# Performance work log

Measured on AMD Instinct MI355X. Metric: run time of the kernel, lower is better.

Reference implementation:

```python
import jax, jax.numpy as jnp
import numpy as np

EPS = 1e-5
DEPTH = 3
NQ = 12


def _bn(x, g, b):
    # BatchNorm1d in training mode: batch statistics, biased variance
    mu = x.mean(0)
    var = x.var(0)
    return (x - mu) / jnp.sqrt(var + EPS) * g + b


def _ln(x, g, b):
    mu = x.mean(-1, keepdims=True)
    var = x.var(-1, keepdims=True)
    return (x - mu) / jnp.sqrt(var + EPS) * g + b


def _apply_1q(s, U, q):
    # s: [B, 2^NQ] complex; U: [2,2] (shared) or [B,2,2] (per-sample); qubit q = q-th MSB
    B = s.shape[0]
    s = s.reshape(B, 2 ** q, 2, -1)
    sub = 'ij,bajc->baic' if U.ndim == 2 else 'bij,bajc->baic'
    return jnp.einsum(sub, U, s).reshape(B, -1)


def _apply_cry(s, theta, c):
    # controlled-Ry(theta): control qubit c, target qubit c+1 (adjacent)
    B = s.shape[0]
    s = s.reshape(B, 2 ** c, 2, 2, -1)
    co = jnp.cos(theta / 2).astype(s.dtype)
    si = jnp.sin(theta / 2).astype(s.dtype)
    s1 = s[:, :, 1]  # control = |1> block
    new1 = jnp.stack([co * s1[:, :, 0] - si * s1[:, :, 1],
                      si * s1[:, :, 0] + co * s1[:, :, 1]], axis=2)
    s = jnp.concatenate([s[:, :, :1], new1[:, :, None]], axis=2)
    return s.reshape(B, -1)


def _measure(s):
    # P(qubit q measures |1>) for each qubit
    p = jnp.abs(s) ** 2  # [B, 2^NQ]
    B = p.shape[0]
    probs = [p.reshape(B, 2 ** q, 2, -1).sum(axis=(1, 3))[:, 1] for q in range(NQ)]
    return jnp.stack(probs, axis=1)  # [B, NQ]


def _rot_mats(rot):
    # fused Rz(rz) @ Ry(ry) @ Rx(rx) for each (depth, qubit) -> [DEPTH, NQ, 2, 2]
    hx, hy, hz = rot[..., 0] / 2, rot[..., 1] / 2, rot[..., 2] / 2
    cx, sx = jnp.cos(hx), jnp.sin(hx)
    Rx = jnp.stack([jnp.stack([cx + 0j, -1j * sx], -1),
                    jnp.stack([-1j * sx, cx + 0j], -1)], -2)
    cy, sy = jnp.cos(hy), jnp.sin(hy)
    Ry = jnp.stack([jnp.stack([cy, -sy], -1),
                    jnp.stack([sy, cy], -1)], -2).astype(jnp.complex64)
    ez = jnp.exp(-1j * hz)
    z0 = jnp.zeros_like(ez)
    Rz = jnp.stack([jnp.stack([ez, z0], -1),
                    jnp.stack([z0, jnp.conj(ez)], -1)], -2)
    return jnp.einsum('...ij,...jk,...kl->...il', Rz, Ry, Rx).astype(jnp.complex64)


def _quantum_layer(x, We, be, gi, bi, rot, ent, Wd, bd, go, bo):
    e = jnp.tanh(_bn(x @ We.T + be, gi, bi))  # [B, NQ]
    nrm = jnp.linalg.norm(e, axis=1, keepdims=True)
    a = jnp.where(nrm > 0, e / nrm, e)        # per-sample L2-normalized amplitudes
    B = x.shape[0]
    s = jnp.zeros((B, 2 ** NQ), jnp.complex64).at[:, 0].set(1.0)
    # amplitude encoding: Ry(2*arcsin(|a|)) then phase pi (sign) if a<0 -> diag(1,-1)@Ry
    ang = 2.0 * jnp.arcsin(jnp.clip(jnp.abs(a), 0.0, 1.0))
    c, si = jnp.cos(ang / 2), jnp.sin(ang / 2)
    sg = jnp.where(a < 0, -1.0, 1.0)
    for q in range(NQ):
        U = jnp.stack([jnp.stack([c[:, q], -si[:, q]], -1),
                       jnp.stack([sg[:, q] * si[:, q], sg[:, q] * c[:, q]], -1)],
                      -2).astype(jnp.complex64)  # [B,2,2]
        s = _apply_1q(s, U, q)
    # parameterized circuit: per-qubit fused Rz.Ry.Rx, then nearest-neighbor CRy chain
    U = _rot_mats(rot)
    for d in range(DEPTH):
        for q in range(NQ):
            s = _apply_1q(s, U[d, q], q)
        for i in range(NQ - 1):
            s = _apply_cry(s, ent[d, i], i)
    m = _measure(s)
    return _bn(m @ Wd.T + bd, go, bo)


def setup_inputs() -> dict:
    key = jax.random.key(0)
    ks = jax.random.split(key, 16)
    B, IN, H1, H2, H3, OUT = 512, 512, 512, 512, 1024, 256

    def lin(k, o, i):
        k1, k2 = jax.random.split(k)
        lim = 1.0 / np.sqrt(i)
        return (jax.random.uniform(k1, (o, i), jnp.float32, -lim, lim),
                jax.random.uniform(k2, (o,), jnp.float32, -lim, lim))

    qWe0, qbe0 = lin(ks[1], NQ, IN)
    qWd0, qbd0 = lin(ks[2], H1, NQ)
    qWe1, qbe1 = lin(ks[3], NQ, H1)
    qWd1, qbd1 = lin(ks[4], H2, NQ)
    W2, b2 = lin(ks[5], H3, H2)
    Wo, bo = lin(ks[6], OUT, H3)
    return {
        'x': jax.random.normal(ks[0], (B, IN), jnp.float32),
        'qWe0': qWe0, 'qbe0': qbe0,
        'qgi0': jnp.ones(NQ), 'qbi0': jnp.zeros(NQ),
        'rot0': 0.1 * jax.random.normal(ks[7], (DEPTH, NQ, 3), jnp.float32),
        'ent0': 0.1 * jax.random.normal(ks[8], (DEPTH, NQ - 1), jnp.float32),
        'qWd0': qWd0, 'qbd0': qbd0,
        'qgo0': jnp.ones(H1), 'qbo0': jnp.zeros(H1),
        'qWe1': qWe1, 'qbe1': qbe1,
        'qgi1': jnp.ones(NQ), 'qbi1': jnp.zeros(NQ),
        'rot1': 0.1 * jax.random.normal(ks[9], (DEPTH, NQ, 3), jnp.float32),
        'ent1': 0.1 * jax.random.normal(ks[10], (DEPTH, NQ - 1), jnp.float32),
        'qWd1': qWd1, 'qbd1': qbd1,
        'qgo1': jnp.ones(H2), 'qbo1': jnp.zeros(H2),
        'W2': W2, 'b2': b2, 'ln2g': jnp.ones(H3), 'ln2b': jnp.zeros(H3),
        'Wo': Wo, 'bo': bo, 'lnog': jnp.ones(OUT), 'lnob': jnp.zeros(OUT),
    }


def reference(x, qWe0, qbe0, qgi0, qbi0, rot0, ent0, qWd0, qbd0, qgo0, qbo0,
              qWe1, qbe1, qgi1, qbi1, rot1, ent1, qWd1, qbd1, qgo1, qbo1,
              W2, b2, ln2g, ln2b, Wo, bo, lnog, lnob):
    h = _quantum_layer(x, qWe0, qbe0, qgi0, qbi0, rot0, ent0, qWd0, qbd0, qgo0, qbo0)
    h = _quantum_layer(h, qWe1, qbe1, qgi1, qbi1, rot1, ent1, qWd1, qbd1, qgo1, qbo1)
    h = jax.nn.relu(_ln(h @ W2.T + b2, ln2g, ln2b))  # classical block (dropout = identity, eval)
    return _ln(h @ Wo.T + bo, lnog, lnob)
```

## Files before the change

kernel.cpp:

```cpp
#include <hip/hip_runtime.h>
#include <math.h>

#define EPS   1e-5f
#define NQ    12
#define DEPTH 3
#define BATCH 512
#define DIM   4096

__device__ inline float2 cmul(float2 a, float2 b) {
    return make_float2(a.x*b.x - a.y*b.y, a.x*b.y + a.y*b.x);
}
__device__ inline float2 cmac2(float2 ua, float2 s, float2 ub, float2 p) {
    return make_float2(ua.x*s.x - ua.y*s.y + ub.x*p.x - ub.y*p.y,
                       ua.x*s.y + ua.y*s.x + ub.x*p.y + ub.y*p.x);
}

__global__ void consts_kernel(const float* __restrict__ rot0, const float* __restrict__ ent0,
                              const float* __restrict__ rot1, const float* __restrict__ ent1,
                              float2* __restrict__ Uc, float2* __restrict__ Cc) {
    int t = threadIdx.x;
    if (t < 72) {
        int layer = t / 36, rem = t % 36, d = rem / 12, q = rem % 12;
        const float* rot = layer ? rot1 : rot0;
        float hx = 0.5f * rot[(d*NQ + q)*3 + 0];
        float hy = 0.5f * rot[(d*NQ + q)*3 + 1];
        float hz = 0.5f * rot[(d*NQ + q)*3 + 2];
        float cx = cosf(hx), sx = sinf(hx);
        float cy = cosf(hy), sy = sinf(hy);
        float2 m00 = make_float2( cy*cx,  sy*sx);
        float2 m01 = make_float2(-sy*cx, -cy*sx);
        float2 m10 = make_float2( sy*cx, -cy*sx);
        float2 m11 = make_float2( cy*cx, -sy*sx);
        float2 ez  = make_float2(cosf(hz), -sinf(hz));
        float2 ezc = make_float2(ez.x, -ez.y);
        float2* U = Uc + t*4;
        U[0] = cmul(ez,  m00);
        U[1] = cmul(ez,  m01);
        U[2] = cmul(ezc, m10);
        U[3] = cmul(ezc, m11);
    } else if (t < 72 + 66) {
        int idx = t - 72, layer = idx / 33, rem = idx % 33;
        const float* ent = layer ? ent1 : ent0;
        float th = 0.5f * ent[rem];
        Cc[idx] = make_float2(cosf(th), sinf(th));
    }
}

__global__ __launch_bounds__(256) void encode_rm_kernel(
        const float* __restrict__ X, const float* __restrict__ We,
        const float* __restrict__ be, float* __restrict__ Yraw) {
    __shared__ float w[NQ][512];
    int tid = threadIdx.x;
    {
        const float4* src = (const float4*)We;
        float4* dst = (float4*)&w[0][0];
        #pragma unroll
        for (int i = tid; i < NQ*512/4; i += 256) dst[i] = src[i];
    }
    __syncthreads();
    int wave = tid >> 6, lane = tid & 63;
    int b = blockIdx.x * 4 + wave;
    const float4* xr = (const float4*)(X + (size_t)b * 512);
    float acc[NQ] = {};
    #pragma unroll
    for (int j = 0; j < 2; ++j) {
        float4 xv = xr[lane + 64*j];
        #pragma unroll
        for (int q = 0; q < NQ; ++q) {
            float4 wv = ((const float4*)&w[q][0])[lane + 64*j];
            acc[q] += xv.x*wv.x + xv.y*wv.y + xv.z*wv.z + xv.w*wv.w;
        }
    }
    #pragma unroll
    for (int q = 0; q < NQ; ++q) {
        float v = acc[q];
        #pragma unroll
        for (int off = 32; off; off >>= 1) v += __shfl_xor(v, off);
        if (lane == q) Yraw[b*NQ + q] = v + be[q];
    }
}

__global__ __launch_bounds__(512) void bn_tanh_kernel(
        const float* __restrict__ Yraw,
        const float* __restrict__ gi, const float* __restrict__ bi,
        float* __restrict__ A) {
    int b = threadIdx.x;
    float v[NQ];
    #pragma unroll
    for (int q = 0; q < NQ; ++q) v[q] = Yraw[b*NQ + q];
    __shared__ float2 red[NQ][8];
    int lane = b & 63, wave = b >> 6;
    #pragma unroll
    for (int q = 0; q < NQ; ++q) {
        float2 t = make_float2(v[q], v[q]*v[q]);
        for (int off = 32; off; off >>= 1) { t.x += __shfl_down(t.x, off); t.y += __shfl_down(t.y, off); }
        if (lane == 0) red[q][wave] = t;
    }
    __syncthreads();
    #pragma unroll
    for (int q = 0; q < NQ; ++q) {
        float s = 0.f, s2 = 0.f;
        #pragma unroll
        for (int wv = 0; wv < 8; ++wv) { s += red[q][wv].x; s2 += red[q][wv].y; }
        float mu  = s  * (1.f/512.f);
        float var = s2 * (1.f/512.f) - mu*mu;
        A[b*NQ + q] = tanhf((v[q] - mu) * rsqrtf(var + EPS) * gi[q] + bi[q]);
    }
}

__device__ inline int swz(int a) { return a ^ ((a >> 4) & 15); }

template<int L> __device__ inline int ampl(int tid, int k) {
    if constexpr (L == 1) return (k << 8) | tid;
    else if constexpr (L == 2) return ((tid & 0xE0) << 4) | (k << 5) | (tid & 0x1F);
    else if constexpr (L == 3) return ((tid & 0xFC) << 4) | (k << 2) | (tid & 3);
    else return (tid << 4) | k;
}

template<int F, int T>
__device__ inline void remap(float2* amp, float2* lds2, int tid) {
    #pragma unroll
    for (int k = 0; k < 16; ++k) lds2[swz(ampl<F>(tid, k))] = amp[k];
    __syncthreads();
    #pragma unroll
    for (int k = 0; k < 16; ++k) amp[k] = lds2[swz(ampl<T>(tid, k))];
    __syncthreads();
}

template<int BP>
__device__ inline void one_q(float2* amp, float2 u00, float2 u01, float2 u10, float2 u11) {
    #pragma unroll
    for (int g = 0; g < 8; ++g) {
        const int j0 = ((g >> BP) << (BP+1)) | (g & ((1<<BP)-1));
        const int j1 = j0 | (1 << BP);
        float2 a0 = amp[j0], a1 = amp[j1];
        amp[j0] = cmac2(u00, a0, u01, a1);
        amp[j1] = cmac2(u10, a0, u11, a1);
    }
}

template<int CB, int TB>
__device__ inline void cry_rr(float2* amp, float co, float si) {
    #pragma unroll
    for (int m = 0; m < 16; ++m) {
        if (((m >> CB) & 1) && !((m >> TB) & 1)) {
            const int j1 = m | (1 << TB);
            float2 a0 = amp[m], a1 = amp[j1];
            amp[m]  = make_float2(co*a0.x - si*a1.x, co*a0.y - si*a1.y);
            amp[j1] = make_float2(si*a0.x + co*a1.x, si*a0.y + co*a1.y);
        }
    }
}

__global__ __launch_bounds__(256) void qsim_kernel(
        const float* __restrict__ A, const float2* __restrict__ UcAll,
        const float2* __restrict__ CcAll, int layer, float* __restrict__ mout) {
    int b = blockIdx.x, tid = threadIdx.x;
    const float2* Uc = UcAll + layer * DEPTH * NQ * 4;
    const float2* Cc = CcAll + layer * DEPTH * (NQ - 1);
    __shared__ float2 lds2[DIM];
    __shared__ float red[NQ][4];

    float av[NQ]; float n2 = 0.f;
    #pragma unroll
    for (int q = 0; q < NQ; ++q) { av[q] = A[b*NQ + q]; n2 += av[q]*av[q]; }
    float scn = (n2 > 0.f) ? rsqrtf(n2) : 1.f;
    float2 v0[NQ], v1[NQ];
    #pragma unroll
    for (int q = 0; q < NQ; ++q) {
        float a  = av[q] * scn;
        float sv = fminf(fabsf(a), 1.f);
        float c  = sqrtf(fmaxf(1.f - sv*sv, 0.f));
        float ss = (a < 0.f) ? -sv : sv;
        const float2* U = Uc + q*4;
        v0[q] = make_float2(U[0].x*c + U[1].x*ss, U[0].y*c + U[1].y*ss);
        v1[q] = make_float2(U[2].x*c + U[3].x*ss, U[2].y*c + U[3].y*ss);
    }
    float2 common = make_float2(1.f, 0.f);
    #pragma unroll
    for (int bb = 0; bb < 8; ++bb)
        common = cmul(common, ((tid >> bb) & 1) ? v1[11-bb] : v0[11-bb]);
    float2 amp[16];
    amp[0] = common;
    #pragma unroll
    for (int m = 0; m < 4; ++m) {
        const int q = 3 - m;
        #pragma unroll
        for (int k = 0; k < (1<<m); ++k) {
            amp[k | (1<<m)] = cmul(amp[k], v1[q]);
            amp[k]          = cmul(amp[k], v0[q]);
        }
    }

    for (int d = 0; d < DEPTH; ++d) {
        const float2* Ud = Uc + d*NQ*4;
        const float2* Cd = Cc + d*(NQ-1);
        if (d > 0) {
            remap<4,1>(amp, lds2, tid);
            one_q<3>(amp, Ud[0],  Ud[1],  Ud[2],  Ud[3]);
            one_q<2>(amp, Ud[4],  Ud[5],  Ud[6],  Ud[7]);
            one_q<1>(amp, Ud[8],  Ud[9],  Ud[10], Ud[11]);
            one_q<0>(amp, Ud[12], Ud[13], Ud[14], Ud[15]);
        }
        cry_rr<3,2>(amp, Cd[0].x, Cd[0].y);
        cry_rr<2,1>(amp, Cd[1].x, Cd[1].y);
        cry_rr<1,0>(amp, Cd[2].x, Cd[2].y);
        remap<1,2>(amp, lds2, tid);
        if (d > 0) {
            one_q<2>(amp, Ud[16], Ud[17], Ud[18], Ud[19]);
            one_q<1>(amp, Ud[20], Ud[21], Ud[22], Ud[23]);
            one_q<0>(amp, Ud[24], Ud[25], Ud[26], Ud[27]);
        }
        cry_rr<3,2>(amp, Cd[3].x, Cd[3].y);
        cry_rr<2,1>(amp, Cd[4].x, Cd[4].y);
        cry_rr<1,0>(amp, Cd[5].x, Cd[5].y);
        remap<2,3>(amp, lds2, tid);
        if (d > 0) {
            one_q<2>(amp, Ud[28], Ud[29], Ud[30], Ud[31]);
            one_q<1>(amp, Ud[32], Ud[33], Ud[34], Ud[35]);
            one_q<0>(amp, Ud[36], Ud[37], Ud[38], Ud[39]);
        }
        cry_rr<3,2>(amp, Cd[6].x, Cd[6].y);
        cry_rr<2,1>(amp, Cd[7].x, Cd[7].y);
        cry_rr<1,0>(amp, Cd[8].x, Cd[8].y);
        remap<3,4>(amp, lds2, tid);
        if (d > 0) {
            one_q<1>(amp, Ud[40], Ud[41], Ud[42], Ud[43]);
            one_q<0>(amp, Ud[44], Ud[45], Ud[46], Ud[47]);
        }
        cry_rr<2,1>(amp, Cd[9].x,  Cd[9].y);
        cry_rr<1,0>(amp, Cd[10].x, Cd[10].y);
    }

    float msum = 0.f, p8 = 0.f, p9 = 0.f, p10 = 0.f, p11 = 0.f;
    #pragma unroll
    for (int k = 0; k < 16; ++k) {
        float m = amp[k].x*amp[k].x + amp[k].y*amp[k].y;
        msum += m;
        if (k & 8) p8  += m;
        if (k & 4) p9  += m;
        if (k & 2) p10 += m;
        if (k & 1) p11 += m;
    }
    int lane = tid & 63, wave = tid >> 6;
    #pragma unroll
    for (int q = 0; q < NQ; ++q) {
        float v;
        if (q < 8)        v = ((tid >> (7-q)) & 1) ? msum : 0.f;
        else if (q == 8)  v = p8;
        else if (q == 9)  v = p9;
        else if (q == 10) v = p10;
        else              v = p11;
        #pragma unroll
        for (int off = 32; off; off >>= 1) v += __shfl_xor(v, off);
        if (lane == 0) red[q][wave] = v;
    }
    __syncthreads();
    if (tid < NQ)
        mout[b*NQ + tid] = red[tid][0] + red[tid][1] + red[tid][2] + red[tid][3];
}

__global__ __launch_bounds__(512) void decode_kernel(
        const float* __restrict__ m, const float* __restrict__ Wd,
        const float* __restrict__ bd, const float* __restrict__ go,
        const float* __restrict__ bo, float* __restrict__ outT) {
    int h = blockIdx.x, b = threadIdx.x;
    __shared__ float sm[BATCH * 13];
    __shared__ float2 red[8];
    for (int idx = b; idx < BATCH * NQ; idx += 512) {
        int bb = idx / NQ, q = idx - bb * NQ;
        sm[bb*13 + q] = m[idx];
    }
    __syncthreads();
    float z = bd[h];
    #pragma unroll
    for (int q = 0; q < NQ; ++q) z += sm[b*13 + q] * Wd[h*NQ + q];

    float2 v = make_float2(z, z*z);
    int lane = b & 63, wave = b >> 6;
    for (int off = 32; off; off >>= 1) { v.x += __shfl_down(v.x, off); v.y += __shfl_down(v.y, off); }
    if (lane == 0) red[wave] = v;
    __syncthreads();
    float s = 0.f, s2 = 0.f;
    #pragma unroll
    for (int wv = 0; wv < 8; ++wv) { s += red[wv].x; s2 += red[wv].y; }
    float mu  = s  * (1.f/512.f);
    float var = s2 * (1.f/512.f) - mu*mu;
    outT[(size_t)h*BATCH + b] = (z - mu) * rsqrtf(var + EPS) * go[h] + bo[h];
}

__global__ __launch_bounds__(256) void transpose512_kernel(
        const float* __restrict__ in, float* __restrict__ out) {
    __shared__ float t[64][68];
    int tx = blockIdx.x & 7, ty = blockIdx.x >> 3;
    int tid = threadIdx.x;
    int c4 = (tid & 15) * 4, rr = tid >> 4;
    #pragma unroll
    for (int i = 0; i < 4; ++i) {
        int h = ty*64 + rr + i*16;
        float4 v = *(const float4*)(in + (size_t)h*512 + tx*64 + c4);
        t[c4+0][rr+i*16] = v.x; t[c4+1][rr+i*16] = v.y;
        t[c4+2][rr+i*16] = v.z; t[c4+3][rr+i*16] = v.w;
    }
    __syncthreads();
    #pragma unroll
    for (int i = 0; i < 4; ++i) {
        int bb = tx*64 + rr + i*16;
        float4 o = *(const float4*)&t[rr+i*16][c4];
        *(float4*)(out + (size_t)bb*512 + ty*64 + c4) = o;
    }
}

__global__ __launch_bounds__(256) void gemm1_kernel(
        const float* __restrict__ AT,
        const float* __restrict__ W,
        float* __restrict__ Cpart) {
    __shared__ float As[2][32][64];
    __shared__ float Bs[2][32][68];
    const int b0 = blockIdx.x * 64, j0 = blockIdx.y * 64;
    const int kbase = blockIdx.z * 256;
    float* C = Cpart + (size_t)blockIdx.z * 512 * 1024;
    const int tid = threadIdx.x;
    const int tr = tid >> 4, tc = tid & 15;
    const int a_kk = tid >> 4, a_f4 = tid & 15;
    const int b_jj = tid >> 3, b_k4 = (tid & 7) * 4;
    float4 ra0, ra1, rb0, rb1;
    float acc[4][4] = {};

    {
        const int k0 = kbase;
        ra0 = *(const float4*)(AT + (size_t)(k0 + a_kk)*512 + b0 + a_f4*4);
        ra1 = *(const float4*)(AT + (size_t)(k0 + a_kk + 16)*512 + b0 + a_f4*4);
        rb0 = *(const float4*)(W + (size_t)(j0 + b_jj)*512 + k0 + b_k4);
        rb1 = *(const float4*)(W + (size_t)(j0 + b_jj + 32)*512 + k0 + b_k4);
        *(float4*)&As[0][a_kk][a_f4*4] = ra0;
        *(float4*)&As[0][a_kk+16][a_f4*4] = ra1;
        Bs[0][b_k4+0][b_jj] = rb0.x; Bs[0][b_k4+1][b_jj] = rb0.y;
        Bs[0][b_k4+2][b_jj] = rb0.z; Bs[0][b_k4+3][b_jj] = rb0.w;
        Bs[0][b_k4+0][b_jj+32] = rb1.x; Bs[0][b_k4+1][b_jj+32] = rb1.y;
        Bs[0][b_k4+2][b_jj+32] = rb1.z; Bs[0][b_k4+3][b_jj+32] = rb1.w;
    }
    __syncthreads();
    for (int s = 0; s < 8; ++s) {
        if (s < 7) {
            const int k0 = kbase + (s+1)*32;
            ra0 = *(const float4*)(AT + (size_t)(k0 + a_kk)*512 + b0 + a_f4*4);
            ra1 = *(const float4*)(AT + (size_t)(k0 + a_kk + 16)*512 + b0 + a_f4*4);
            rb0 = *(const float4*)(W + (size_t)(j0 + b_jj)*512 + k0 + b_k4);
            rb1 = *(const float4*)(W + (size_t)(j0 + b_jj + 32)*512 + k0 + b_k4);
        }
        const int bf = s & 1;
        #pragma unroll
        for (int kk = 0; kk < 32; ++kk) {
            float4 a  = *(const float4*)&As[bf][kk][tr*4];
            float4 bv = *(const float4*)&Bs[bf][kk][tc*4];
            acc[0][0] += a.x*bv.x; acc[0][1] += a.x*bv.y; acc[0][2] += a.x*bv.z; acc[0][3] += a.x*bv.w;
            acc[1][0] += a.y*bv.x; acc[1][1] += a.y*bv.y; acc[1][2] += a.y*bv.z; acc[1][3] += a.y*bv.w;
            acc[2][0] += a.z*bv.x; acc[2][1] += a.z*bv.y; acc[2][2] += a.z*bv.z; acc[2][3] += a.z*bv.w;
            acc[3][0] += a.w*bv.x; acc[3][1] += a.w*bv.y; acc[3][2] += a.w*bv.z; acc[3][3] += a.w*bv.w;
        }
        if (s < 7) {
            const int nb = bf ^ 1;
            *(float4*)&As[nb][a_kk][a_f4*4] = ra0;
            *(float4*)&As[nb][a_kk+16][a_f4*4] = ra1;
            Bs[nb][b_k4+0][b_jj] = rb0.x; Bs[nb][b_k4+1][b_jj] = rb0.y;
            Bs[nb][b_k4+2][b_jj] = rb0.z; Bs[nb][b_k4+3][b_jj] = rb0.w;
            Bs[nb][b_k4+0][b_jj+32] = rb1.x; Bs[nb][b_k4+1][b_jj+32] = rb1.y;
            Bs[nb][b_k4+2][b_jj+32] = rb1.z; Bs[nb][b_k4+3][b_jj+32] = rb1.w;
        }
        __syncthreads();
    }
    #pragma unroll
    for (int r = 0; r < 4; ++r) {
        float4 o = make_float4(acc[r][0], acc[r][1], acc[r][2], acc[r][3]);
        *(float4*)(C + (size_t)(b0 + tr*4 + r)*1024 + j0 + tc*4) = o;
    }
}

__global__ __launch_bounds__(256) void gemm2_kernel(
        const float* __restrict__ Amat,
        const float* __restrict__ W,
        float* __restrict__ Cpart) {
    __shared__ float As[2][32][68];
    __shared__ float Bs[2][32][68];
    const int b0 = blockIdx.x * 64, j0 = blockIdx.y * 64;
    const int kbase = blockIdx.z * 128;
    float* C = Cpart + (size_t)blockIdx.z * 512 * 256;
    const int tid = threadIdx.x;
    const int tr = tid >> 4, tc = tid & 15;
    const int l_r = tid >> 3, l_k4 = (tid & 7) * 4;
    float4 ra0, ra1, rb0, rb1;
    float acc[4][4] = {};

    {
        const int k0 = kbase;
        ra0 = *(const float4*)(Amat + (size_t)(b0 + l_r)*1024 + k0 + l_k4);
        ra1 = *(const float4*)(Amat + (size_t)(b0 + l_r + 32)*1024 + k0 + l_k4);
        rb0 = *(const float4*)(W + (size_t)(j0 + l_r)*1024 + k0 + l_k4);
        rb1 = *(const float4*)(W + (size_t)(j0 + l_r + 32)*1024 + k0 + l_k4);
        As[0][l_k4+0][l_r] = ra0.x; As[0][l_k4+1][l_r] = ra0.y;
        As[0][l_k4+2][l_r] = ra0.z; As[0][l_k4+3][l_r] = ra0.w;
        As[0][l_k4+0][l_r+32] = ra1.x; As[0][l_k4+1][l_r+32] = ra1.y;
        As[0][l_k4+2][l_r+32] = ra1.z; As[0][l_k4+3][l_r+32] = ra1.w;
        Bs[0][l_k4+0][l_r] = rb0.x; Bs[0][l_k4+1][l_r] = rb0.y;
        Bs[0][l_k4+2][l_r] = rb0.z; Bs[0][l_k4+3][l_r] = rb0.w;
        Bs[0][l_k4+0][l_r+32] = rb1.x; Bs[0][l_k4+1][l_r+32] = rb1.y;
        Bs[0][l_k4+2][l_r+32] = rb1.z; Bs[0][l_k4+3][l_r+32] = rb1.w;
    }
    __syncthreads();
    for (int s = 0; s < 4; ++s) {
        if (s < 3) {
            const int k0 = kbase + (s+1)*32;
            ra0 = *(const float4*)(Amat + (size_t)(b0 + l_r)*1024 + k0 + l_k4);
            ra1 = *(const float4*)(Amat + (size_t)(b0 + l_r + 32)*1024 + k0 + l_k4);
            rb0 = *(const float4*)(W + (size_t)(j0 + l_r)*1024 + k0 + l_k4);
            rb1 = *(const float4*)(W + (size_t)(j0 + l_r + 32)*1024 + k0 + l_k4);
        }
        const int bf = s & 1;
        #pragma unroll
        for (int kk = 0; kk < 32; ++kk) {
            float4 a  = *(const float4*)&As[bf][kk][tr*4];
            float4 bv = *(const float4*)&Bs[bf][kk][tc*4];
            acc[0][0] += a.x*bv.x; acc[0][1] += a.x*bv.y; acc[0][2] += a.x*bv.z; acc[0][3] += a.x*bv.w;
            acc[1][0] += a.y*bv.x; acc[1][1] += a.y*bv.y; acc[1][2] += a.y*bv.z; acc[1][3] += a.y*bv.w;
            acc[2][0] += a.z*bv.x; acc[2][1] += a.z*bv.y; acc[2][2] += a.z*bv.z; acc[2][3] += a.z*bv.w;
            acc[3][0] += a.w*bv.x; acc[3][1] += a.w*bv.y; acc[3][2] += a.w*bv.z; acc[3][3] += a.w*bv.w;
        }
        if (s < 3) {
            const int nb = bf ^ 1;
            As[nb][l_k4+0][l_r] = ra0.x; As[nb][l_k4+1][l_r] = ra0.y;
            As[nb][l_k4+2][l_r] = ra0.z; As[nb][l_k4+3][l_r] = ra0.w;
            As[nb][l_k4+0][l_r+32] = ra1.x; As[nb][l_k4+1][l_r+32] = ra1.y;
            As[nb][l_k4+2][l_r+32] = ra1.z; As[nb][l_k4+3][l_r+32] = ra1.w;
            Bs[nb][l_k4+0][l_r] = rb0.x; Bs[nb][l_k4+1][l_r] = rb0.y;
            Bs[nb][l_k4+2][l_r] = rb0.z; Bs[nb][l_k4+3][l_r] = rb0.w;
            Bs[nb][l_k4+0][l_r+32] = rb1.x; Bs[nb][l_k4+1][l_r+32] = rb1.y;
            Bs[nb][l_k4+2][l_r+32] = rb1.z; Bs[nb][l_k4+3][l_r+32] = rb1.w;
        }
        __syncthreads();
    }
    #pragma unroll
    for (int r = 0; r < 4; ++r) {
        float4 o = make_float4(acc[r][0], acc[r][1], acc[r][2], acc[r][3]);
        *(float4*)(C + (size_t)(b0 + tr*4 + r)*256 + j0 + tc*4) = o;
    }
}

__global__ __launch_bounds__(256) void ln_relu_kernel(
        const float* __restrict__ P,
        const float* __restrict__ bias,
        const float* __restrict__ g, const float* __restrict__ be,
        float* __restrict__ Y) {
    int b = blockIdx.x, tid = threadIdx.x;
    __shared__ float2 red[4];
    const float* p0 = P + (size_t)b * 1024;
    const float* p1 = P + 524288 + (size_t)b * 1024;
    float v0 = p0[tid]     + p1[tid]     + bias[tid];
    float v1 = p0[tid+256] + p1[tid+256] + bias[tid+256];
    float v2 = p0[tid+512] + p1[tid+512] + bias[tid+512];
    float v3 = p0[tid+768] + p1[tid+768] + bias[tid+768];
    float2 v = make_float2(v0+v1+v2+v3, v0*v0+v1*v1+v2*v2+v3*v3);
    int lane = tid & 63, wave = tid >> 6;
    for (int off = 32; off; off >>= 1) { v.x += __shfl_down(v.x, off); v.y += __shfl_down(v.y, off); }
    if (lane == 0) red[wave] = v;
    __syncthreads();
    float s = 0.f, s2 = 0.f;
    #pragma unroll
    for (int wv = 0; wv < 4; ++wv) { s += red[wv].x; s2 += red[wv].y; }
    float mu  = s  * (1.f/1024.f);
    float var = s2 * (1.f/1024.f) - mu*mu;
    float inv = rsqrtf(var + EPS);
    float* yr = Y + (size_t)b * 1024;
    yr[tid]     = fmaxf((v0-mu)*inv*g[tid]     + be[tid],     0.f);
    yr[tid+256] = fmaxf((v1-mu)*inv*g[tid+256] + be[tid+256], 0.f);
    yr[tid+512] = fmaxf((v2-mu)*inv*g[tid+512] + be[tid+512], 0.f);
    yr[tid+768] = fmaxf((v3-mu)*inv*g[tid+768] + be[tid+768], 0.f);
}

__global__ __launch_bounds__(256) void ln_out_kernel(
        const float* __restrict__ P,
        const float* __restrict__ bias,
        const float* __restrict__ g, const float* __restrict__ be,
        float* __restrict__ Y) {
    int b = blockIdx.x, tid = threadIdx.x;
    __shared__ float2 red[4];
    float v0 = bias[tid];
    #pragma unroll
    for (int z = 0; z < 8; ++z) v0 += P[(size_t)z*131072 + (size_t)b*256 + tid];
    float2 v = make_float2(v0, v0*v0);
    int lane = tid & 63, wave = tid >> 6;
    for (int off = 32; off; off >>= 1) { v.x += __shfl_down(v.x, off); v.y += __shfl_down(v.y, off); }
    if (lane == 0) red[wave] = v;
    __syncthreads();
    float s = 0.f, s2 = 0.f;
    #pragma unroll
    for (int wv = 0; wv < 4; ++wv) { s += red[wv].x; s2 += red[wv].y; }
    float mu  = s  * (1.f/256.f);
    float var = s2 * (1.f/256.f) - mu*mu;
    Y[(size_t)b*256 + tid] = (v0 - mu) * rsqrtf(var + EPS) * g[tid] + be[tid];
}

extern "C" void kernel_launch(void* const* d_in, const int* in_sizes, int n_in,
                              void* d_out, int out_size, void* d_ws, size_t ws_size,
                              hipStream_t stream) {
    const float* x    = (const float*)d_in[0];
    const float* qWe0 = (const float*)d_in[1];
    const float* qbe0 = (const float*)d_in[2];
    const float* qgi0 = (const float*)d_in[3];
    const float* qbi0 = (const float*)d_in[4];
    const float* rot0 = (const float*)d_in[5];
    const float* ent0 = (const float*)d_in[6];
    const float* qWd0 = (const float*)d_in[7];
    const float* qbd0 = (const float*)d_in[8];
    const float* qgo0 = (const float*)d_in[9];
    const float* qbo0 = (const float*)d_in[10];
    const float* qWe1 = (const float*)d_in[11];
    const float* qbe1 = (const float*)d_in[12];
    const float* qgi1 = (const float*)d_in[13];
    const float* qbi1 = (const float*)d_in[14];
    const float* rot1 = (const float*)d_in[15];
    const float* ent1 = (const float*)d_in[16];
    const float* qWd1 = (const float*)d_in[17];
    const float* qbd1 = (const float*)d_in[18];
    const float* qgo1 = (const float*)d_in[19];
    const float* qbo1 = (const float*)d_in[20];
    const float* W2   = (const float*)d_in[21];
    const float* b2   = (const float*)d_in[22];
    const float* ln2g = (const float*)d_in[23];
    const float* ln2b = (const float*)d_in[24];
    const float* Wo   = (const float*)d_in[25];
    const float* bo   = (const float*)d_in[26];
    const float* lnog = (const float*)d_in[27];
    const float* lnob = (const float*)d_in[28];
    float* out = (float*)d_out;
    float* ws  = (float*)d_ws;

    float2* Uc = (float2*)ws;
    float2* Cc = Uc + 288;
    float* A0   = ws + 1024;
    float* m0   = ws + 7168;
    float* A1   = ws + 13312;
    float* m1   = ws + 19456;
    float* Yraw = ws + 25600;
    float* h1T  = ws + 32768;
    float* h1   = ws + 294912;
    float* h2T  = ws + 32768;
    float* t3p  = ws + 557056;
    float* t3n  = ws + 1605632;
    float* t4p  = ws + 557056;

    hipLaunchKernelGGL(consts_kernel, dim3(1), dim3(256), 0, stream,
                       rot0, ent0, rot1, ent1, Uc, Cc);

    hipLaunchKernelGGL(encode_rm_kernel, dim3(128), dim3(256), 0, stream,
                       x, qWe0, qbe0, Yraw);
    hipLaunchKernelGGL(bn_tanh_kernel, dim3(1), dim3(512), 0, stream,
                       Yraw, qgi0, qbi0, A0);
    hipLaunchKernelGGL(qsim_kernel, dim3(512), dim3(256), 0, stream,
                       A0, Uc, Cc, 0, m0);
    hipLaunchKernelGGL(decode_kernel, dim3(512), dim3(512), 0, stream,
                       m0, qWd0, qbd0, qgo0, qbo0, h1T);
    hipLaunchKernelGGL(transpose512_kernel, dim3(64), dim3(256), 0, stream,
                       h1T, h1);

    hipLaunchKernelGGL(encode_rm_kernel, dim3(128), dim3(256), 0, stream,
                       h1, qWe1, qbe1, Yraw);
    hipLaunchKernelGGL(bn_tanh_kernel, dim3(1), dim3(512), 0, stream,
                       Yraw, qgi1, qbi1, A1);
    hipLaunchKernelGGL(qsim_kernel, dim3(512), dim3(256), 0, stream,
                       A1, Uc, Cc, 1, m1);
    hipLaunchKernelGGL(decode_kernel, dim3(512), dim3(512), 0, stream,
                       m1, qWd1, qbd1, qgo1, qbo1, h2T);

    hipLaunchKernelGGL(gemm1_kernel, dim3(8, 16, 2), dim3(256), 0, stream,
                       h2T, W2, t3p);
    hipLaunchKernelGGL(ln_relu_kernel, dim3(512), dim3(256), 0, stream,
                       t3p, b2, ln2g, ln2b, t3n);
    hipLaunchKernelGGL(gemm2_kernel, dim3(8, 4, 8), dim3(256), 0, stream,
                       t3n, Wo, t4p);
    hipLaunchKernelGGL(ln_out_kernel, dim3(512), dim3(256), 0, stream,
                       t4p, bo, lnog, lnob, out);
}
```

Measured before the change: 235.1 us.

## Fuse whole pipeline into one cooperative persistent mega-kernel with grid syncs

Replaces the chain of about fourteen kernel launches with a single cooperative kernel of 512 blocks. Stages are separated by grid-wide synchronisation, and the batch-norm statistics are folded into each qsim block. The aim is to remove per-launch overhead and the tiny single-block serial stages. If the cooperative launch fails, the code falls back to the multi-kernel path. The risks are the cost of grid barriers and a requirement that all 512 blocks be co-resident.

```diff
diff --git a/kernel.cpp b/kernel.cpp
--- a/kernel.cpp
+++ b/kernel.cpp
@@ -1,5 +1,8 @@
 #include <hip/hip_runtime.h>
+#include <hip/hip_cooperative_groups.h>
 #include <math.h>
+
+namespace cg = cooperative_groups;
 
 #define EPS   1e-5f
 #define NQ    12
@@ -15,10 +18,150 @@
                        ua.x*s.y + ua.y*s.x + ub.x*p.y + ub.y*p.x);
 }
 
-__global__ void consts_kernel(const float* __restrict__ rot0, const float* __restrict__ ent0,
-                              const float* __restrict__ rot1, const float* __restrict__ ent1,
-                              float2* __restrict__ Uc, float2* __restrict__ Cc) {
-    int t = threadIdx.x;
+__device__ inline int swz(int a) { return a ^ ((a >> 4) & 15); }
+
+template<int L> __device__ inline int ampl(int tid, int k) {
+    if constexpr (L == 1) return (k << 8) | tid;
+    else if constexpr (L == 2) return ((tid & 0xE0) << 4) | (k << 5) | (tid & 0x1F);
+    else if constexpr (L == 3) return ((tid & 0xFC) << 4) | (k << 2) | (tid & 3);
+    else return (tid << 4) | k;
+}
+
+template<int F, int T>
+__device__ inline void remap(float2* amp, float2* lds2, int tid) {
+    #pragma unroll
+    for (int k = 0; k < 16; ++k) lds2[swz(ampl<F>(tid, k))] = amp[k];
+    __syncthreads();
+    #pragma unroll
+    for (int k = 0; k < 16; ++k) amp[k] = lds2[swz(ampl<T>(tid, k))];
+    __syncthreads();
+}
+
+template<int BP>
+__device__ inline void one_q(float2* amp, float2 u00, float2 u01, float2 u10, float2 u11) {
+    #pragma unroll
+    for (int g = 0; g < 8; ++g) {
+        const int j0 = ((g >> BP) << (BP+1)) | (g & ((1<<BP)-1));
+        const int j1 = j0 | (1 << BP);
+        float2 a0 = amp[j0], a1 = amp[j1];
+        amp[j0] = cmac2(u00, a0, u01, a1);
+        amp[j1] = cmac2(u10, a0, u11, a1);
+    }
+}
+
+template<int CB, int TB>
+__device__ inline void cry_rr(float2* amp, float co, float si) {
+    #pragma unroll
+    for (int m = 0; m < 16; ++m) {
+        if (((m >> CB) & 1) && !((m >> TB) & 1)) {
+            const int j1 = m | (1 << TB);
+            float2 a0 = amp[m], a1 = amp[j1];
+            amp[m]  = make_float2(co*a0.x - si*a1.x, co*a0.y - si*a1.y);
+            amp[j1] = make_float2(si*a0.x + co*a1.x, si*a0.y + co*a1.y);
+        }
+    }
+}
+
+__device__ void qsim_core(float2* amp, float2* lds2, float* redm,
+                          const float2* Uc, const float2* Cc,
+                          int tid, int b, float* mout) {
+    for (int d = 0; d < DEPTH; ++d) {
+        const float2* Ud = Uc + d*NQ*4;
+        const float2* Cd = Cc + d*(NQ-1);
+        if (d > 0) {
+            remap<4,1>(amp, lds2, tid);
+            one_q<3>(amp, Ud[0],  Ud[1],  Ud[2],  Ud[3]);
+            one_q<2>(amp, Ud[4],  Ud[5],  Ud[6],  Ud[7]);
+            one_q<1>(amp, Ud[8],  Ud[9],  Ud[10], Ud[11]);
+            one_q<0>(amp, Ud[12], Ud[13], Ud[14], Ud[15]);
+        }
+        cry_rr<3,2>(amp, Cd[0].x, Cd[0].y);
+        cry_rr<2,1>(amp, Cd[1].x, Cd[1].y);
+        cry_rr<1,0>(amp, Cd[2].x, Cd[2].y);
+        remap<1,2>(amp, lds2, tid);
+        if (d > 0) {
+            one_q<2>(amp, Ud[16], Ud[17], Ud[18], Ud[19]);
+            one_q<1>(amp, Ud[20], Ud[21], Ud[22], Ud[23]);
+            one_q<0>(amp, Ud[24], Ud[25], Ud[26], Ud[27]);
+        }
+        cry_rr<3,2>(amp, Cd[3].x, Cd[3].y);
+        cry_rr<2,1>(amp, Cd[4].x, Cd[4].y);
+        cry_rr<1,0>(amp, Cd[5].x, Cd[5].y);
+        remap<2,3>(amp, lds2, tid);
+        if (d > 0) {
+            one_q<2>(amp, Ud[28], Ud[29], Ud[30], Ud[31]);
+            one_q<1>(amp, Ud[32], Ud[33], Ud[34], Ud[35]);
+            one_q<0>(amp, Ud[36], Ud[37], Ud[38], Ud[39]);
+        }
+        cry_rr<3,2>(amp, Cd[6].x, Cd[6].y);
+        cry_rr<2,1>(amp, Cd[7].x, Cd[7].y);
+        cry_rr<1,0>(amp, Cd[8].x, Cd[8].y);
+        remap<3,4>(amp, lds2, tid);
+        if (d > 0) {
+            one_q<1>(amp, Ud[40], Ud[41], Ud[42], Ud[43]);
+            one_q<0>(amp, Ud[44], Ud[45], Ud[46], Ud[47]);
+        }
+        cry_rr<2,1>(amp, Cd[9].x,  Cd[9].y);
+        cry_rr<1,0>(amp, Cd[10].x, Cd[10].y);
+    }
+    float msum = 0.f, p8 = 0.f, p9 = 0.f, p10 = 0.f, p11 = 0.f;
+    #pragma unroll
+    for (int k = 0; k < 16; ++k) {
+        float m = amp[k].x*amp[k].x + amp[k].y*amp[k].y;
+        msum += m;
+        if (k & 8) p8  += m;
+        if (k & 4) p9  += m;
+        if (k & 2) p10 += m;
+        if (k & 1) p11 += m;
+    }
+    int lane = tid & 63, wave = tid >> 6;
+    #pragma unroll
+    for (int q = 0; q < NQ; ++q) {
+        float v;
+        if (q < 8)        v = ((tid >> (7-q)) & 1) ? msum : 0.f;
+        else if (q == 8)  v = p8;
+        else if (q == 9)  v = p9;
+        else if (q == 10) v = p10;
+        else              v = p11;
+        #pragma unroll
+        for (int off = 32; off; off >>= 1) v += __shfl_xor(v, off);
+        if (lane == 0) redm[q*4 + wave] = v;
+    }
+    __syncthreads();
+    if (tid < NQ)
+        mout[b*NQ + tid] = redm[tid*4] + redm[tid*4+1] + redm[tid*4+2] + redm[tid*4+3];
+}
+
+__device__ void qsim_init(float2* amp, const float* a, const float2* Uc, int tid) {
+    float2 v0[NQ], v1[NQ];
+    #pragma unroll
+    for (int q = 0; q < NQ; ++q) {
+        float sv = fminf(fabsf(a[q]), 1.f);
+        float c  = sqrtf(fmaxf(1.f - sv*sv, 0.f));
+        float ss = (a[q] < 0.f) ? -sv : sv;
+        const float2* U = Uc + q*4;
+        v0[q] = make_float2(U[0].x*c + U[1].x*ss, U[0].y*c + U[1].y*ss);
+        v1[q] = make_float2(U[2].x*c + U[3].x*ss, U[2].y*c + U[3].y*ss);
+    }
+    float2 common = make_float2(1.f, 0.f);
+    #pragma unroll
+    for (int bb = 0; bb < 8; ++bb)
+        common = cmul(common, ((tid >> bb) & 1) ? v1[11-bb] : v0[11-bb]);
+    amp[0] = common;
+    #pragma unroll
+    for (int m = 0; m < 4; ++m) {
+        const int q = 3 - m;
+        #pragma unroll
+        for (int k = 0; k < (1<<m); ++k) {
+            amp[k | (1<<m)] = cmul(amp[k], v1[q]);
+            amp[k]          = cmul(amp[k], v0[q]);
+        }
+    }
+}
+
+__device__ void consts_body(int t,
+        const float* rot0, const float* ent0, const float* rot1, const float* ent1,
+        float2* Uc, float2* Cc) {
     if (t < 72) {
         int layer = t / 36, rem = t % 36, d = rem / 12, q = rem % 12;
         const float* rot = layer ? rot1 : rot0;
@@ -46,287 +189,184 @@
     }
 }
 
-__global__ __launch_bounds__(256) void encode_rm_kernel(
-        const float* __restrict__ X, const float* __restrict__ We,
-        const float* __restrict__ be, float* __restrict__ Yraw) {
-    __shared__ float w[NQ][512];
-    int tid = threadIdx.x;
+struct MegaParams {
+    const float *x;
+    const float *qWe0, *qbe0, *qgi0, *qbi0, *rot0, *ent0, *qWd0, *qbd0, *qgo0, *qbo0;
+    const float *qWe1, *qbe1, *qgi1, *qbi1, *rot1, *ent1, *qWd1, *qbd1, *qgo1, *qbo1;
+    const float *W2, *b2, *ln2g, *ln2b, *Wo, *bo, *lnog, *lnob;
+    float2 *Uc, *Cc;
+    float *Yraw0, *m0, *Yraw1, *m1, *h1T, *h2T, *t3p, *t3n, *t4p, *out;
+};
+
+#define SMEM_BYTES 37888
+
+__device__ void dev_encode_row(const float* X, const float* We, const float* be,
+                               float* Yraw, int b, int tid, char* smem) {
+    float (*w)[512] = (float(*)[512])smem;
     {
         const float4* src = (const float4*)We;
-        float4* dst = (float4*)&w[0][0];
-        #pragma unroll
-        for (int i = tid; i < NQ*512/4; i += 256) dst[i] = src[i];
-    }
-    __syncthreads();
-    int wave = tid >> 6, lane = tid & 63;
-    int b = blockIdx.x * 4 + wave;
-    const float4* xr = (const float4*)(X + (size_t)b * 512);
-    float acc[NQ] = {};
-    #pragma unroll
-    for (int j = 0; j < 2; ++j) {
-        float4 xv = xr[lane + 64*j];
-        #pragma unroll
-        for (int q = 0; q < NQ; ++q) {
-            float4 wv = ((const float4*)&w[q][0])[lane + 64*j];
-            acc[q] += xv.x*wv.x + xv.y*wv.y + xv.z*wv.z + xv.w*wv.w;
-        }
-    }
+        float4* dst = (float4*)smem;
+        #pragma unroll
+        for (int i = tid; i < NQ*128; i += 256) dst[i] = src[i];
+    }
+    __syncthreads();
+    float2 xv = *(const float2*)(X + (size_t)b*512 + tid*2);
+    float acc[NQ];
+    #pragma unroll
+    for (int q = 0; q < NQ; ++q)
+        acc[q] = xv.x * w[q][tid*2] + xv.y * w[q][tid*2+1];
+    int lane = tid & 63, wave = tid >> 6;
+    float* red = (float*)(smem + 24576);
     #pragma unroll
     for (int q = 0; q < NQ; ++q) {
         float v = acc[q];
         #pragma unroll
         for (int off = 32; off; off >>= 1) v += __shfl_xor(v, off);
-        if (lane == q) Yraw[b*NQ + q] = v + be[q];
-    }
-}
-
-__global__ __launch_bounds__(512) void bn_tanh_kernel(
-        const float* __restrict__ Yraw,
-        const float* __restrict__ gi, const float* __restrict__ bi,
-        float* __restrict__ A) {
-    int b = threadIdx.x;
-    float v[NQ];
-    #pragma unroll
-    for (int q = 0; q < NQ; ++q) v[q] = Yraw[b*NQ + q];
-    __shared__ float2 red[NQ][8];
-    int lane = b & 63, wave = b >> 6;
+        if (lane == 0) red[wave*NQ + q] = v;
+    }
+    __syncthreads();
+    if (tid < NQ)
+        Yraw[b*NQ + tid] = red[tid] + red[NQ+tid] + red[2*NQ+tid] + red[3*NQ+tid] + be[tid];
+}
+
+__device__ void dev_qsim(const float* Yraw, const float* gi, const float* bi,
+                         const float2* UcL, const float2* CcL,
+                         float* mout, float* zeroY, int blk, int tid, char* smem) {
+    float2* lds2 = (float2*)smem;
+    float*  sred = (float*)(smem + 32768);
+    if (zeroY && tid < NQ) zeroY[blk*NQ + tid] = 0.f;
+    float sum[NQ] = {}, sq[NQ] = {};
+    const float4* Y4 = (const float4*)Yraw;
+    #pragma unroll
+    for (int j = 0; j < 6; ++j) {
+        float4 v = Y4[tid*6 + j];
+        int q0 = (j*4) % 12;
+        sum[q0+0]+=v.x; sq[q0+0]+=v.x*v.x;
+        sum[q0+1]+=v.y; sq[q0+1]+=v.y*v.y;
+        sum[q0+2]+=v.z; sq[q0+2]+=v.z*v.z;
+        sum[q0+3]+=v.w; sq[q0+3]+=v.w*v.w;
+    }
+    int lane = tid & 63, wave = tid >> 6;
     #pragma unroll
     for (int q = 0; q < NQ; ++q) {
-        float2 t = make_float2(v[q], v[q]*v[q]);
-        for (int off = 32; off; off >>= 1) { t.x += __shfl_down(t.x, off); t.y += __shfl_down(t.y, off); }
-        if (lane == 0) red[q][wave] = t;
-    }
-    __syncthreads();
+        #pragma unroll
+        for (int off = 32; off; off >>= 1) {
+            sum[q] += __shfl_xor(sum[q], off);
+            sq[q]  += __shfl_xor(sq[q],  off);
+        }
+    }
+    if (lane == 0) {
+        #pragma unroll
+        for (int q = 0; q < NQ; ++q) {
+            sred[wave*24 + q]      = sum[q];
+            sred[wave*24 + 12 + q] = sq[q];
+        }
+    }
+    __syncthreads();
+    float a[NQ]; float n2 = 0.f;
+    const float* yr = Yraw + blk*NQ;
     #pragma unroll
     for (int q = 0; q < NQ; ++q) {
-        float s = 0.f, s2 = 0.f;
-        #pragma unroll
-        for (int wv = 0; wv < 8; ++wv) { s += red[q][wv].x; s2 += red[q][wv].y; }
+        float s  = sred[q]      + sred[24+q] + sred[48+q] + sred[72+q];
+        float s2 = sred[12+q]   + sred[36+q] + sred[60+q] + sred[84+q];
         float mu  = s  * (1.f/512.f);
         float var = s2 * (1.f/512.f) - mu*mu;
-        A[b*NQ + q] = tanhf((v[q] - mu) * rsqrtf(var + EPS) * gi[q] + bi[q]);
-    }
-}
-
-__device__ inline int swz(int a) { return a ^ ((a >> 4) & 15); }
-
-template<int L> __device__ inline int ampl(int tid, int k) {
-    if constexpr (L == 1) return (k << 8) | tid;
-    else if constexpr (L == 2) return ((tid & 0xE0) << 4) | (k << 5) | (tid & 0x1F);
-    else if constexpr (L == 3) return ((tid & 0xFC) << 4) | (k << 2) | (tid & 3);
-    else return (tid << 4) | k;
-}
-
-template<int F, int T>
-__device__ inline void remap(float2* amp, float2* lds2, int tid) {
-    #pragma unroll
-    for (int k = 0; k < 16; ++k) lds2[swz(ampl<F>(tid, k))] = amp[k];
-    __syncthreads();
-    #pragma unroll
-    for (int k = 0; k < 16; ++k) amp[k] = lds2[swz(ampl<T>(tid, k))];
-    __syncthreads();
-}
-
-template<int BP>
-__device__ inline void one_q(float2* amp, float2 u00, float2 u01, float2 u10, float2 u11) {
-    #pragma unroll
-    for (int g = 0; g < 8; ++g) {
-        const int j0 = ((g >> BP) << (BP+1)) | (g & ((1<<BP)-1));
-        const int j1 = j0 | (1 << BP);
-        float2 a0 = amp[j0], a1 = amp[j1];
-        amp[j0] = cmac2(u00, a0, u01, a1);
-        amp[j1] = cmac2(u10, a0, u11, a1);
-    }
-}
-
-template<int CB, int TB>
-__device__ inline void cry_rr(float2* amp, float co, float si) {
-    #pragma unroll
-    for (int m = 0; m < 16; ++m) {
-        if (((m >> CB) & 1) && !((m >> TB) & 1)) {
-            const int j1 = m | (1 << TB);
-            float2 a0 = amp[m], a1 = amp[j1];
-            amp[m]  = make_float2(co*a0.x - si*a1.x, co*a0.y - si*a1.y);
-            amp[j1] = make_float2(si*a0.x + co*a1.x, si*a0.y + co*a1.y);
-        }
-    }
-}
-
-__global__ __launch_bounds__(256) void qsim_kernel(
-        const float* __restrict__ A, const float2* __restrict__ UcAll,
-        const float2* __restrict__ CcAll, int layer, float* __restrict__ mout) {
-    int b = blockIdx.x, tid = threadIdx.x;
-    const float2* Uc = UcAll + layer * DEPTH * NQ * 4;
-    const float2* Cc = CcAll + layer * DEPTH * (NQ - 1);
-    __shared__ float2 lds2[DIM];
-    __shared__ float red[NQ][4];
-
-    float av[NQ]; float n2 = 0.f;
-    #pragma unroll
-    for (int q = 0; q < NQ; ++q) { av[q] = A[b*NQ + q]; n2 += av[q]*av[q]; }
+        float val = (yr[q] - mu) * rsqrtf(var + EPS) * gi[q] + bi[q];
+        a[q] = tanhf(val);
+        n2 += a[q]*a[q];
+    }
     float scn = (n2 > 0.f) ? rsqrtf(n2) : 1.f;
-    float2 v0[NQ], v1[NQ];
+    #pragma unroll
+    for (int q = 0; q < NQ; ++q) a[q] *= scn;
+    __syncthreads();
+    float2 amp[16];
+    qsim_init(amp, a, UcL, tid);
+    qsim_core(amp, lds2, sred, UcL, CcL, tid, blk, mout);
+}
+
+__device__ void dev_decode(const float* m, const float* Wd, const float* bd,
+                           const float* go, const float* bo, float* outT,
+                           int h, int tid, char* smem) {
+    float* sm = (float*)smem;
+    float2* red = (float2*)(smem + 512*13*4);
+    const float4* m4 = (const float4*)m;
+    for (int f4 = tid; f4 < 1536; f4 += 256) {
+        float4 v = m4[f4];
+        int base = f4*4; int row = base/12; int q = base - row*12;
+        float* dst = sm + row*13 + q;
+        dst[0]=v.x; dst[1]=v.y; dst[2]=v.z; dst[3]=v.w;
+    }
+    __syncthreads();
+    float wreg[NQ];
+    #pragma unroll
+    for (int q = 0; q < NQ; ++q) wreg[q] = Wd[h*NQ + q];
+    float bdv = bd[h];
+    float z0 = bdv, z1 = bdv;
     #pragma unroll
     for (int q = 0; q < NQ; ++q) {
-        float a  = av[q] * scn;
-        float sv = fminf(fabsf(a), 1.f);
-        float c  = sqrtf(fmaxf(1.f - sv*sv, 0.f));
-        float ss = (a < 0.f) ? -sv : sv;
-        const float2* U = Uc + q*4;
-        v0[q] = make_float2(U[0].x*c + U[1].x*ss, U[0].y*c + U[1].y*ss);
-        v1[q] = make_float2(U[2].x*c + U[3].x*ss, U[2].y*c + U[3].y*ss);
-    }
-    float2 common = make_float2(1.f, 0.f);
-    #pragma unroll
-    for (int bb = 0; bb < 8; ++bb)
-        common = cmul(common, ((tid >> bb) & 1) ? v1[11-bb] : v0[11-bb]);
-    float2 amp[16];
-    amp[0] = common;
-    #pragma unroll
-    for (int m = 0; m < 4; ++m) {
-        const int q = 3 - m;
-        #pragma unroll
-        for (int k = 0; k < (1<<m); ++k) {
-            amp[k | (1<<m)] = cmul(amp[k], v1[q]);
-            amp[k]          = cmul(amp[k], v0[q]);
-        }
-    }
-
-    for (int d = 0; d < DEPTH; ++d) {
-        const float2* Ud = Uc + d*NQ*4;
-        const float2* Cd = Cc + d*(NQ-1);
-        if (d > 0) {
-            remap<4,1>(amp, lds2, tid);
-            one_q<3>(amp, Ud[0],  Ud[1],  Ud[2],  Ud[3]);
-            one_q<2>(amp, Ud[4],  Ud[5],  Ud[6],  Ud[7]);
-            one_q<1>(amp, Ud[8],  Ud[9],  Ud[10], Ud[11]);
-            one_q<0>(amp, Ud[12], Ud[13], Ud[14], Ud[15]);
-        }
-        cry_rr<3,2>(amp, Cd[0].x, Cd[0].y);
-        cry_rr<2,1>(amp, Cd[1].x, Cd[1].y);
-        cry_rr<1,0>(amp, Cd[2].x, Cd[2].y);
-        remap<1,2>(amp, lds2, tid);
-        if (d > 0) {
-            one_q<2>(amp, Ud[16], Ud[17], Ud[18], Ud[19]);
-            one_q<1>(amp, Ud[20], Ud[21], Ud[22], Ud[23]);
-            one_q<0>(amp, Ud[24], Ud[25], Ud[26], Ud[27]);
-        }
-        cry_rr<3,2>(amp, Cd[3].x, Cd[3].y);
-        cry_rr<2,1>(amp, Cd[4].x, Cd[4].y);
-        cry_rr<1,0>(amp, Cd[5].x, Cd[5].y);
-        remap<2,3>(amp, lds2, tid);
-        if (d > 0) {
-            one_q<2>(amp, Ud[28], Ud[29], Ud[30], Ud[31]);
-            one_q<1>(amp, Ud[32], Ud[33], Ud[34], Ud[35]);
-            one_q<0>(amp, Ud[36], Ud[37], Ud[38], Ud[39]);
-        }
-        cry_rr<3,2>(amp, Cd[6].x, Cd[6].y);
-        cry_rr<2,1>(amp, Cd[7].x, Cd[7].y);
-        cry_rr<1,0>(amp, Cd[8].x, Cd[8].y);
-        remap<3,4>(amp, lds2, tid);
-        if (d > 0) {
-            one_q<1>(amp, Ud[40], Ud[41], Ud[42], Ud[43]);
-            one_q<0>(amp, Ud[44], Ud[45], Ud[46], Ud[47]);
-        }
-        cry_rr<2,1>(amp, Cd[9].x,  Cd[9].y);
-        cry_rr<1,0>(amp, Cd[10].x, Cd[10].y);
-    }
-
-    float msum = 0.f, p8 = 0.f, p9 = 0.f, p10 = 0.f, p11 = 0.f;
-    #pragma unroll
-    for (int k = 0; k < 16; ++k) {
-        float m = amp[k].x*amp[k].x + amp[k].y*amp[k].y;
-        msum += m;
-        if (k & 8) p8  += m;
-        if (k & 4) p9  += m;
-        if (k & 2) p10 += m;
-        if (k & 1) p11 += m;
-    }
+        z0 += sm[tid*13 + q]       * wreg[q];
+        z1 += sm[(tid+256)*13 + q] * wreg[q];
+    }
+    float2 v = make_float2(z0+z1, z0*z0 + z1*z1);
     int lane = tid & 63, wave = tid >> 6;
-    #pragma unroll
-    for (int q = 0; q < NQ; ++q) {
-        float v;
-        if (q < 8)        v = ((tid >> (7-q)) & 1) ? msum : 0.f;
-        else if (q == 8)  v = p8;
-        else if (q == 9)  v = p9;
-        else if (q == 10) v = p10;
-        else              v = p11;
-        #pragma unroll
-        for (int off = 32; off; off >>= 1) v += __shfl_xor(v, off);
-        if (lane == 0) red[q][wave] = v;
-    }
-    __syncthreads();
-    if (tid < NQ)
-        mout[b*NQ + tid] = red[tid][0] + red[tid][1] + red[tid][2] + red[tid][3];
-}
-
-__global__ __launch_bounds__(512) void decode_kernel(
-        const float* __restrict__ m, const float* __restrict__ Wd,
-        const float* __restrict__ bd, const float* __restrict__ go,
-        const float* __restrict__ bo, float* __restrict__ outT) {
-    int h = blockIdx.x, b = threadIdx.x;
-    __shared__ float sm[BATCH * 13];
-    __shared__ float2 red[8];
-    for (int idx = b; idx < BATCH * NQ; idx += 512) {
-        int bb = idx / NQ, q = idx - bb * NQ;
-        sm[bb*13 + q] = m[idx];
-    }
-    __syncthreads();
-    float z = bd[h];
-    #pragma unroll
-    for (int q = 0; q < NQ; ++q) z += sm[b*13 + q] * Wd[h*NQ + q];
-
-    float2 v = make_float2(z, z*z);
-    int lane = b & 63, wave = b >> 6;
     for (int off = 32; off; off >>= 1) { v.x += __shfl_down(v.x, off); v.y += __shfl_down(v.y, off); }
     if (lane == 0) red[wave] = v;
     __syncthreads();
-    float s = 0.f, s2 = 0.f;
-    #pragma unroll
-    for (int wv = 0; wv < 8; ++wv) { s += red[wv].x; s2 += red[wv].y; }
+    float s = red[0].x + red[1].x + red[2].x + red[3].x;
+    float s2 = red[0].y + red[1].y + red[2].y + red[3].y;
     float mu  = s  * (1.f/512.f);
     float var = s2 * (1.f/512.f) - mu*mu;
-    outT[(size_t)h*BATCH + b] = (z - mu) * rsqrtf(var + EPS) * go[h] + bo[h];
-}
-
-__global__ __launch_bounds__(256) void transpose512_kernel(
-        const float* __restrict__ in, float* __restrict__ out) {
-    __shared__ float t[64][68];
-    int tx = blockIdx.x & 7, ty = blockIdx.x >> 3;
-    int tid = threadIdx.x;
-    int c4 = (tid & 15) * 4, rr = tid >> 4;
-    #pragma unroll
-    for (int i = 0; i < 4; ++i) {
-        int h = ty*64 + rr + i*16;
-        float4 v = *(const float4*)(in + (size_t)h*512 + tx*64 + c4);
-        t[c4+0][rr+i*16] = v.x; t[c4+1][rr+i*16] = v.y;
-        t[c4+2][rr+i*16] = v.z; t[c4+3][rr+i*16] = v.w;
-    }
-    __syncthreads();
-    #pragma unroll
-    for (int i = 0; i < 4; ++i) {
-        int bb = tx*64 + rr + i*16;
-        float4 o = *(const float4*)&t[rr+i*16][c4];
-        *(float4*)(out + (size_t)bb*512 + ty*64 + c4) = o;
-    }
-}
-
-__global__ __launch_bounds__(256) void gemm1_kernel(
-        const float* __restrict__ AT,
-        const float* __restrict__ W,
-        float* __restrict__ Cpart) {
-    __shared__ float As[2][32][64];
-    __shared__ float Bs[2][32][68];
-    const int b0 = blockIdx.x * 64, j0 = blockIdx.y * 64;
-    const int kbase = blockIdx.z * 256;
-    float* C = Cpart + (size_t)blockIdx.z * 512 * 1024;
-    const int tid = threadIdx.x;
+    float inv = rsqrtf(var + EPS) * go[h];
+    float bov = bo[h];
+    outT[(size_t)h*BATCH + tid]       = (z0 - mu) * inv + bov;
+    outT[(size_t)h*BATCH + tid + 256] = (z1 - mu) * inv + bov;
+}
+
+__device__ void dev_encode1(const float* h1T, const float* We, const float* be,
+                            float* Yraw1, int blk, int tid, char* smem) {
+    float (*w)[512] = (float(*)[512])smem;
+    float* red = (float*)(smem + 24576);
+    {
+        const float4* src = (const float4*)We;
+        float4* dst = (float4*)smem;
+        #pragma unroll
+        for (int i = tid; i < NQ*128; i += 256) dst[i] = src[i];
+    }
+    __syncthreads();
+    int kc = blk >> 3, bc = blk & 7;
+    int bl = tid & 63, hg = tid >> 6;
+    int b = bc*64 + bl;
+    float acc[NQ] = {};
+    #pragma unroll
+    for (int i = 0; i < 16; ++i) {
+        int h = kc*64 + hg*16 + i;
+        float xv = h1T[(size_t)h*512 + b];
+        #pragma unroll
+        for (int q = 0; q < NQ; ++q) acc[q] += xv * w[q][h];
+    }
+    #pragma unroll
+    for (int q = 0; q < NQ; ++q) red[(hg*64 + bl)*NQ + q] = acc[q];
+    __syncthreads();
+    for (int i = tid; i < 64*NQ; i += 256) {
+        int bl2 = i / NQ, q = i - bl2*NQ;
+        float v = red[bl2*NQ+q] + red[(64+bl2)*NQ+q] + red[(128+bl2)*NQ+q] + red[(192+bl2)*NQ+q];
+        if (kc == 0) v += be[q];
+        atomicAdd(&Yraw1[(size_t)(bc*64 + bl2)*NQ + q], v);
+    }
+}
+
+__device__ void dev_gemm1(const float* AT, const float* W, float* Cpart,
+                          int blk, int tid, char* smem) {
+    float (*As)[32][64] = (float(*)[32][64])smem;
+    float (*Bs)[32][68] = (float(*)[32][68])(smem + 16384);
+    const int bx = blk & 7, by = (blk >> 3) & 15, bz = blk >> 7;
+    const int b0 = bx*64, j0 = by*64, kbase = bz*128;
+    float* C = Cpart + (size_t)bz * 512 * 1024;
     const int tr = tid >> 4, tc = tid & 15;
     const int a_kk = tid >> 4, a_f4 = tid & 15;
     const int b_jj = tid >> 3, b_k4 = (tid & 7) * 4;
     float4 ra0, ra1, rb0, rb1;
     float acc[4][4] = {};
-
     {
         const int k0 = kbase;
         ra0 = *(const float4*)(AT + (size_t)(k0 + a_kk)*512 + b0 + a_f4*4);
@@ -341,6 +381,342 @@
         Bs[0][b_k4+2][b_jj+32] = rb1.z; Bs[0][b_k4+3][b_jj+32] = rb1.w;
     }
     __syncthreads();
+    for (int s = 0; s < 4; ++s) {
+        if (s < 3) {
+            const int k0 = kbase + (s+1)*32;
+            ra0 = *(const float4*)(AT + (size_t)(k0 + a_kk)*512 + b0 + a_f4*4);
+            ra1 = *(const float4*)(AT + (size_t)(k0 + a_kk + 16)*512 + b0 + a_f4*4);
+            rb0 = *(const float4*)(W + (size_t)(j0 + b_jj)*512 + k0 + b_k4);
+            rb1 = *(const float4*)(W + (size_t)(j0 + b_jj + 32)*512 + k0 + b_k4);
+        }
+        const int bf = s & 1;
+        #pragma unroll
+        for (int kk = 0; kk < 32; ++kk) {
+            float4 a  = *(const float4*)&As[bf][kk][tr*4];
+            float4 bv = *(const float4*)&Bs[bf][kk][tc*4];
+            acc[0][0] += a.x*bv.x; acc[0][1] += a.x*bv.y; acc[0][2] += a.x*bv.z; acc[0][3] += a.x*bv.w;
+            acc[1][0] += a.y*bv.x; acc[1][1] += a.y*bv.y; acc[1][2] += a.y*bv.z; acc[1][3] += a.y*bv.w;
+            acc[2][0] += a.z*bv.x; acc[2][1] += a.z*bv.y; acc[2][2] += a.z*bv.z; acc[2][3] += a.z*bv.w;
+            acc[3][0] += a.w*bv.x; acc[3][1] += a.w*bv.y; acc[3][2] += a.w*bv.z; acc[3][3] += a.w*bv.w;
+        }
+        if (s < 3) {
+            const int nb = bf ^ 1;
+            *(float4*)&As[nb][a_kk][a_f4*4] = ra0;
+            *(float4*)&As[nb][a_kk+16][a_f4*4] = ra1;
+            Bs[nb][b_k4+0][b_jj] = rb0.x; Bs[nb][b_k4+1][b_jj] = rb0.y;
+            Bs[nb][b_k4+2][b_jj] = rb0.z; Bs[nb][b_k4+3][b_jj] = rb0.w;
+            Bs[nb][b_k4+0][b_jj+32] = rb1.x; Bs[nb][b_k4+1][b_jj+32] = rb1.y;
+            Bs[nb][b_k4+2][b_jj+32] = rb1.z; Bs[nb][b_k4+3][b_jj+32] = rb1.w;
+        }
+        __syncthreads();
+    }
+    #pragma unroll
+    for (int r = 0; r < 4; ++r) {
+        float4 o = make_float4(acc[r][0], acc[r][1], acc[r][2], acc[r][3]);
+        *(float4*)(C + (size_t)(b0 + tr*4 + r)*1024 + j0 + tc*4) = o;
+    }
+}
+
+__device__ void dev_ln_relu(const float* P, const float* bias, const float* g,
+                            const float* be, float* Y, int b, int tid, char* smem) {
+    float2* red = (float2*)smem;
+    float v[4];
+    #pragma unroll
+    for (int j = 0; j < 4; ++j) {
+        int col = tid + j*256;
+        float t = bias[col];
+        #pragma unroll
+        for (int z = 0; z < 4; ++z) t += P[(size_t)z*524288 + (size_t)b*1024 + col];
+        v[j] = t;
+    }
+    float2 r = make_float2(v[0]+v[1]+v[2]+v[3],
+                           v[0]*v[0]+v[1]*v[1]+v[2]*v[2]+v[3]*v[3]);
+    int lane = tid & 63, wave = tid >> 6;
+    for (int off = 32; off; off >>= 1) { r.x += __shfl_down(r.x, off); r.y += __shfl_down(r.y, off); }
+    if (lane == 0) red[wave] = r;
+    __syncthreads();
+    float s = red[0].x + red[1].x + red[2].x + red[3].x;
+    float s2 = red[0].y + red[1].y + red[2].y + red[3].y;
+    float mu  = s  * (1.f/1024.f);
+    float var = s2 * (1.f/1024.f) - mu*mu;
+    float inv = rsqrtf(var + EPS);
+    float* yr = Y + (size_t)b * 1024;
+    #pragma unroll
+    for (int j = 0; j < 4; ++j) {
+        int col = tid + j*256;
+        yr[col] = fmaxf((v[j]-mu)*inv*g[col] + be[col], 0.f);
+    }
+}
+
+__device__ void dev_gemm2(const float* Amat, const float* W, float* Cpart,
+                          int blk, int tid, char* smem) {
+    float (*As)[32][36] = (float(*)[32][36])smem;
+    float (*Bs)[32][68] = (float(*)[32][68])(smem + 9216);
+    const int bx = blk & 15, by = (blk >> 4) & 3, bz = blk >> 6;
+    const int b0 = bx*32, j0 = by*64, kbase = bz*128;
+    float* C = Cpart + (size_t)bz * 512 * 256;
+    const int tr = tid >> 4, tc = tid & 15;
+    const int l_r = tid >> 3, l_k4 = (tid & 7) * 4;
+    float4 ra0, rb0, rb1;
+    float acc[2][4] = {};
+    {
+        const int k0 = kbase;
+        ra0 = *(const float4*)(Amat + (size_t)(b0 + l_r)*1024 + k0 + l_k4);
+        rb0 = *(const float4*)(W + (size_t)(j0 + l_r)*1024 + k0 + l_k4);
+        rb1 = *(const float4*)(W + (size_t)(j0 + l_r + 32)*1024 + k0 + l_k4);
+        As[0][l_k4+0][l_r] = ra0.x; As[0][l_k4+1][l_r] = ra0.y;
+        As[0][l_k4+2][l_r] = ra0.z; As[0][l_k4+3][l_r] = ra0.w;
+        Bs[0][l_k4+0][l_r] = rb0.x; Bs[0][l_k4+1][l_r] = rb0.y;
+        Bs[0][l_k4+2][l_r] = rb0.z; Bs[0][l_k4+3][l_r] = rb0.w;
+        Bs[0][l_k4+0][l_r+32] = rb1.x; Bs[0][l_k4+1][l_r+32] = rb1.y;
+        Bs[0][l_k4+2][l_r+32] = rb1.z; Bs[0][l_k4+3][l_r+32] = rb1.w;
+    }
+    __syncthreads();
+    for (int s = 0; s < 4; ++s) {
+        if (s < 3) {
+            const int k0 = kbase + (s+1)*32;
+            ra0 = *(const float4*)(Amat + (size_t)(b0 + l_r)*1024 + k0 + l_k4);
+            rb0 = *(const float4*)(W + (size_t)(j0 + l_r)*1024 + k0 + l_k4);
+            rb1 = *(const float4*)(W + (size_t)(j0 + l_r + 32)*1024 + k0 + l_k4);
+        }
+        const int bf = s & 1;
+        #pragma unroll
+        for (int kk = 0; kk < 32; ++kk) {
+            float a0 = As[bf][kk][tr*2], a1 = As[bf][kk][tr*2+1];
+            float4 bv = *(const float4*)&Bs[bf][kk][tc*4];
+            acc[0][0] += a0*bv.x; acc[0][1] += a0*bv.y; acc[0][2] += a0*bv.z; acc[0][3] += a0*bv.w;
+            acc[1][0] += a1*bv.x; acc[1][1] += a1*bv.y; acc[1][2] += a1*bv.z; acc[1][3] += a1*bv.w;
+        }
+        if (s < 3) {
+            const int nb = bf ^ 1;
+            As[nb][l_k4+0][l_r] = ra0.x; As[nb][l_k4+1][l_r] = ra0.y;
+            As[nb][l_k4+2][l_r] = ra0.z; As[nb][l_k4+3][l_r] = ra0.w;
+            Bs[nb][l_k4+0][l_r] = rb0.x; Bs[nb][l_k4+1][l_r] = rb0.y;
+            Bs[nb][l_k4+2][l_r] = rb0.z; Bs[nb][l_k4+3][l_r] = rb0.w;
+            Bs[nb][l_k4+0][l_r+32] = rb1.x; Bs[nb][l_k4+1][l_r+32] = rb1.y;
+            Bs[nb][l_k4+2][l_r+32] = rb1.z; Bs[nb][l_k4+3][l_r+32] = rb1.w;
+        }
+        __syncthreads();
+    }
+    #pragma unroll
+    for (int r = 0; r < 2; ++r) {
+        float4 o = make_float4(acc[r][0], acc[r][1], acc[r][2], acc[r][3]);
+        *(float4*)(C + (size_t)(b0 + tr*2 + r)*256 + j0 + tc*4) = o;
+    }
+}
+
+__device__ void dev_ln_out(const float* P, const float* bias, const float* g,
+                           const float* be, float* Y, int b, int tid, char* smem) {
+    float2* red = (float2*)smem;
+    float v0 = bias[tid];
+    #pragma unroll
+    for (int z = 0; z < 8; ++z) v0 += P[(size_t)z*131072 + (size_t)b*256 + tid];
+    float2 v = make_float2(v0, v0*v0);
+    int lane = tid & 63, wave = tid >> 6;
+    for (int off = 32; off; off >>= 1) { v.x += __shfl_down(v.x, off); v.y += __shfl_down(v.y, off); }
+    if (lane == 0) red[wave] = v;
+    __syncthreads();
+    float s = red[0].x + red[1].x + red[2].x + red[3].x;
+    float s2 = red[0].y + red[1].y + red[2].y + red[3].y;
+    float mu  = s  * (1.f/256.f);
+    float var = s2 * (1.f/256.f) - mu*mu;
+    Y[(size_t)b*256 + tid] = (v0 - mu) * rsqrtf(var + EPS) * g[tid] + be[tid];
+}
+
+__global__ void __launch_bounds__(256, 2) mega_kernel(MegaParams p) {
+    cg::grid_group grid = cg::this_grid();
+    __shared__ __align__(16) char smem[SMEM_BYTES];
+    const int blk = blockIdx.x, tid = threadIdx.x;
+
+    dev_encode_row(p.x, p.qWe0, p.qbe0, p.Yraw0, blk, tid, smem);
+    if (blk == 511) consts_body(tid, p.rot0, p.ent0, p.rot1, p.ent1, p.Uc, p.Cc);
+    grid.sync();
+    dev_qsim(p.Yraw0, p.qgi0, p.qbi0, p.Uc, p.Cc, p.m0, p.Yraw1, blk, tid, smem);
+    grid.sync();
+    dev_decode(p.m0, p.qWd0, p.qbd0, p.qgo0, p.qbo0, p.h1T, blk, tid, smem);
+    grid.sync();
+    if (blk < 64) dev_encode1(p.h1T, p.qWe1, p.qbe1, p.Yraw1, blk, tid, smem);
+    grid.sync();
+    dev_qsim(p.Yraw1, p.qgi1, p.qbi1, p.Uc + DEPTH*NQ*4, p.Cc + DEPTH*(NQ-1),
+             p.m1, nullptr, blk, tid, smem);
+    grid.sync();
+    dev_decode(p.m1, p.qWd1, p.qbd1, p.qgo1, p.qbo1, p.h2T, blk, tid, smem);
+    grid.sync();
+    dev_gemm1(p.h2T, p.W2, p.t3p, blk, tid, smem);
+    grid.sync();
+    dev_ln_relu(p.t3p, p.b2, p.ln2g, p.ln2b, p.t3n, blk, tid, smem);
+    grid.sync();
+    dev_gemm2(p.t3n, p.Wo, p.t4p, blk, tid, smem);
+    grid.sync();
+    dev_ln_out(p.t4p, p.bo, p.lnog, p.lnob, p.out, blk, tid, smem);
+}
+
+__global__ void consts_kernel(const float* __restrict__ rot0, const float* __restrict__ ent0,
+                              const float* __restrict__ rot1, const float* __restrict__ ent1,
+                              float2* __restrict__ Uc, float2* __restrict__ Cc) {
+    consts_body(threadIdx.x, rot0, ent0, rot1, ent1, Uc, Cc);
+}
+
+__global__ __launch_bounds__(256) void encode_rm_kernel(
+        const float* __restrict__ X, const float* __restrict__ We,
+        const float* __restrict__ be, float* __restrict__ Yraw) {
+    __shared__ float w[NQ][512];
+    int tid = threadIdx.x;
+    {
+        const float4* src = (const float4*)We;
+        float4* dst = (float4*)&w[0][0];
+        #pragma unroll
+        for (int i = tid; i < NQ*512/4; i += 256) dst[i] = src[i];
+    }
+    __syncthreads();
+    int wave = tid >> 6, lane = tid & 63;
+    int b = blockIdx.x * 4 + wave;
+    const float4* xr = (const float4*)(X + (size_t)b * 512);
+    float acc[NQ] = {};
+    #pragma unroll
+    for (int j = 0; j < 2; ++j) {
+        float4 xv = xr[lane + 64*j];
+        #pragma unroll
+        for (int q = 0; q < NQ; ++q) {
+            float4 wv = ((const float4*)&w[q][0])[lane + 64*j];
+            acc[q] += xv.x*wv.x + xv.y*wv.y + xv.z*wv.z + xv.w*wv.w;
+        }
+    }
+    #pragma unroll
+    for (int q = 0; q < NQ; ++q) {
+        float v = acc[q];
+        #pragma unroll
+        for (int off = 32; off; off >>= 1) v += __shfl_xor(v, off);
+        if (lane == q) Yraw[b*NQ + q] = v + be[q];
+    }
+}
+
+__global__ __launch_bounds__(512) void bn_tanh_kernel(
+        const float* __restrict__ Yraw,
+        const float* __restrict__ gi, const float* __restrict__ bi,
+        float* __restrict__ A) {
+    int b = threadIdx.x;
+    float v[NQ];
+    #pragma unroll
+    for (int q = 0; q < NQ; ++q) v[q] = Yraw[b*NQ + q];
+    __shared__ float2 red[NQ][8];
+    int lane = b & 63, wave = b >> 6;
+    #pragma unroll
+    for (int q = 0; q < NQ; ++q) {
+        float2 t = make_float2(v[q], v[q]*v[q]);
+        for (int off = 32; off; off >>= 1) { t.x += __shfl_down(t.x, off); t.y += __shfl_down(t.y, off); }
+        if (lane == 0) red[q][wave] = t;
+    }
+    __syncthreads();
+    #pragma unroll
+    for (int q = 0; q < NQ; ++q) {
+        float s = 0.f, s2 = 0.f;
+        #pragma unroll
+        for (int wv = 0; wv < 8; ++wv) { s += red[q][wv].x; s2 += red[q][wv].y; }
+        float mu  = s  * (1.f/512.f);
+        float var = s2 * (1.f/512.f) - mu*mu;
+        A[b*NQ + q] = tanhf((v[q] - mu) * rsqrtf(var + EPS) * gi[q] + bi[q]);
+    }
+}
+
+__global__ __launch_bounds__(256) void qsim_kernel(
+        const float* __restrict__ A, const float2* __restrict__ UcAll,
+        const float2* __restrict__ CcAll, int layer, float* __restrict__ mout) {
+    int b = blockIdx.x, tid = threadIdx.x;
+    const float2* Uc = UcAll + layer * DEPTH * NQ * 4;
+    const float2* Cc = CcAll + layer * DEPTH * (NQ - 1);
+    __shared__ float2 lds2[DIM];
+    __shared__ float redm[NQ * 4];
+    float a[NQ]; float n2 = 0.f;
+    #pragma unroll
+    for (int q = 0; q < NQ; ++q) { a[q] = A[b*NQ + q]; n2 += a[q]*a[q]; }
+    float scn = (n2 > 0.f) ? rsqrtf(n2) : 1.f;
+    #pragma unroll
+    for (int q = 0; q < NQ; ++q) a[q] *= scn;
+    float2 amp[16];
+    qsim_init(amp, a, Uc, tid);
+    qsim_core(amp, lds2, redm, Uc, Cc, tid, b, mout);
+}
+
+__global__ __launch_bounds__(512) void decode_kernel(
+        const float* __restrict__ m, const float* __restrict__ Wd,
+        const float* __restrict__ bd, const float* __restrict__ go,
+        const float* __restrict__ bo, float* __restrict__ outT) {
+    int h = blockIdx.x, b = threadIdx.x;
+    __shared__ float sm[BATCH * 13];
+    __shared__ float2 red[8];
+    for (int idx = b; idx < BATCH * NQ; idx += 512) {
+        int bb = idx / NQ, q = idx - bb * NQ;
+        sm[bb*13 + q] = m[idx];
+    }
+    __syncthreads();
+    float z = bd[h];
+    #pragma unroll
+    for (int q = 0; q < NQ; ++q) z += sm[b*13 + q] * Wd[h*NQ + q];
+    float2 v = make_float2(z, z*z);
+    int lane = b & 63, wave = b >> 6;
+    for (int off = 32; off; off >>= 1) { v.x += __shfl_down(v.x, off); v.y += __shfl_down(v.y, off); }
+    if (lane == 0) red[wave] = v;
+    __syncthreads();
+    float s = 0.f, s2 = 0.f;
+    #pragma unroll
+    for (int wv = 0; wv < 8; ++wv) { s += red[wv].x; s2 += red[wv].y; }
+    float mu  = s  * (1.f/512.f);
+    float var = s2 * (1.f/512.f) - mu*mu;
+    outT[(size_t)h*BATCH + b] = (z - mu) * rsqrtf(var + EPS) * go[h] + bo[h];
+}
+
+__global__ __launch_bounds__(256) void transpose512_kernel(
+        const float* __restrict__ in, float* __restrict__ out) {
+    __shared__ float t[64][68];
+    int tx = blockIdx.x & 7, ty = blockIdx.x >> 3;
+    int tid = threadIdx.x;
+    int c4 = (tid & 15) * 4, rr = tid >> 4;
+    #pragma unroll
+    for (int i = 0; i < 4; ++i) {
+        int h = ty*64 + rr + i*16;
+        float4 v = *(const float4*)(in + (size_t)h*512 + tx*64 + c4);
+        t[c4+0][rr+i*16] = v.x; t[c4+1][rr+i*16] = v.y;
+        t[c4+2][rr+i*16] = v.z; t[c4+3][rr+i*16] = v.w;
+    }
+    __syncthreads();
+    #pragma unroll
+    for (int i = 0; i < 4; ++i) {
+        int bb = tx*64 + rr + i*16;
+        float4 o = *(const float4*)&t[rr+i*16][c4];
+        *(float4*)(out + (size_t)bb*512 + ty*64 + c4) = o;
+    }
+}
+
+__global__ __launch_bounds__(256) void gemm1_fb_kernel(
+        const float* __restrict__ AT, const float* __restrict__ W,
+        float* __restrict__ Cpart) {
+    __shared__ __align__(16) char smem[SMEM_BYTES];
+    float (*As)[32][64] = (float(*)[32][64])smem;
+    float (*Bs)[32][68] = (float(*)[32][68])(smem + 16384);
+    const int b0 = blockIdx.x * 64, j0 = blockIdx.y * 64;
+    const int kbase = blockIdx.z * 256;
+    float* C = Cpart + (size_t)blockIdx.z * 512 * 1024;
+    const int tid = threadIdx.x;
+    const int tr = tid >> 4, tc = tid & 15;
+    const int a_kk = tid >> 4, a_f4 = tid & 15;
+    const int b_jj = tid >> 3, b_k4 = (tid & 7) * 4;
+    float4 ra0, ra1, rb0, rb1;
+    float acc[4][4] = {};
+    {
+        const int k0 = kbase;
+        ra0 = *(const float4*)(AT + (size_t)(k0 + a_kk)*512 + b0 + a_f4*4);
+        ra1 = *(const float4*)(AT + (size_t)(k0 + a_kk + 16)*512 + b0 + a_f4*4);
+        rb0 = *(const float4*)(W + (size_t)(j0 + b_jj)*512 + k0 + b_k4);
+        rb1 = *(const float4*)(W + (size_t)(j0 + b_jj + 32)*512 + k0 + b_k4);
+        *(float4*)&As[0][a_kk][a_f4*4] = ra0;
+        *(float4*)&As[0][a_kk+16][a_f4*4] = ra1;
+        Bs[0][b_k4+0][b_jj] = rb0.x; Bs[0][b_k4+1][b_jj] = rb0.y;
+        Bs[0][b_k4+2][b_jj] = rb0.z; Bs[0][b_k4+3][b_jj] = rb0.w;
+        Bs[0][b_k4+0][b_jj+32] = rb1.x; Bs[0][b_k4+1][b_jj+32] = rb1.y;
+        Bs[0][b_k4+2][b_jj+32] = rb1.z; Bs[0][b_k4+3][b_jj+32] = rb1.w;
+    }
+    __syncthreads();
     for (int s = 0; s < 8; ++s) {
         if (s < 7) {
             const int k0 = kbase + (s+1)*32;
@@ -377,78 +753,8 @@
     }
 }
 
-__global__ __launch_bounds__(256) void gemm2_kernel(
-        const float* __restrict__ Amat,
-        const float* __restrict__ W,
-        float* __restrict__ Cpart) {
-    __shared__ float As[2][32][68];
-    __shared__ float Bs[2][32][68];
-    const int b0 = blockIdx.x * 64, j0 = blockIdx.y * 64;
-    const int kbase = blockIdx.z * 128;
-    float* C = Cpart + (size_t)blockIdx.z * 512 * 256;
-    const int tid = threadIdx.x;
-    const int tr = tid >> 4, tc = tid & 15;
-    const int l_r = tid >> 3, l_k4 = (tid & 7) * 4;
-    float4 ra0, ra1, rb0, rb1;
-    float acc[4][4] = {};
-
-    {
-        const int k0 = kbase;
-        ra0 = *(const float4*)(Amat + (size_t)(b0 + l_r)*1024 + k0 + l_k4);
-        ra1 = *(const float4*)(Amat + (size_t)(b0 + l_r + 32)*1024 + k0 + l_k4);
-        rb0 = *(const float4*)(W + (size_t)(j0 + l_r)*1024 + k0 + l_k4);
-        rb1 = *(const float4*)(W + (size_t)(j0 + l_r + 32)*1024 + k0 + l_k4);
-        As[0][l_k4+0][l_r] = ra0.x; As[0][l_k4+1][l_r] = ra0.y;
-        As[0][l_k4+2][l_r] = ra0.z; As[0][l_k4+3][l_r] = ra0.w;
-        As[0][l_k4+0][l_r+32] = ra1.x; As[0][l_k4+1][l_r+32] = ra1.y;
-        As[0][l_k4+2][l_r+32] = ra1.z; As[0][l_k4+3][l_r+32] = ra1.w;
-        Bs[0][l_k4+0][l_r] = rb0.x; Bs[0][l_k4+1][l_r] = rb0.y;
-        Bs[0][l_k4+2][l_r] = rb0.z; Bs[0][l_k4+3][l_r] = rb0.w;
-        Bs[0][l_k4+0][l_r+32] = rb1.x; Bs[0][l_k4+1][l_r+32] = rb1.y;
-        Bs[0][l_k4+2][l_r+32] = rb1.z; Bs[0][l_k4+3][l_r+32] = rb1.w;
-    }
-    __syncthreads();
-    for (int s = 0; s < 4; ++s) {
-        if (s < 3) {
-            const int k0 = kbase + (s+1)*32;
-            ra0 = *(const float4*)(Amat + (size_t)(b0 + l_r)*1024 + k0 + l_k4);
-            ra1 = *(const float4*)(Amat + (size_t)(b0 + l_r + 32)*1024 + k0 + l_k4);
-            rb0 = *(const float4*)(W + (size_t)(j0 + l_r)*1024 + k0 + l_k4);
-            rb1 = *(const float4*)(W + (size_t)(j0 + l_r + 32)*1024 + k0 + l_k4);
-        }
-        const int bf = s & 1;
-        #pragma unroll
-        for (int kk = 0; kk < 32; ++kk) {
-            float4 a  = *(const float4*)&As[bf][kk][tr*4];
-            float4 bv = *(const float4*)&Bs[bf][kk][tc*4];
-            acc[0][0] += a.x*bv.x; acc[0][1] += a.x*bv.y; acc[0][2] += a.x*bv.z; acc[0][3] += a.x*bv.w;
-            acc[1][0] += a.y*bv.x; acc[1][1] += a.y*bv.y; acc[1][2] += a.y*bv.z; acc[1][3] += a.y*bv.w;
-            acc[2][0] += a.z*bv.x; acc[2][1] += a.z*bv.y; acc[2][2] += a.z*bv.z; acc[2][3] += a.z*bv.w;
-            acc[3][0] += a.w*bv.x; acc[3][1] += a.w*bv.y; acc[3][2] += a.w*bv.z; acc[3][3] += a.w*bv.w;
-        }
-        if (s < 3) {
-            const int nb = bf ^ 1;
-            As[nb][l_k4+0][l_r] = ra0.x; As[nb][l_k4+1][l_r] = ra0.y;
-            As[nb][l_k4+2][l_r] = ra0.z; As[nb][l_k4+3][l_r] = ra0.w;
-            As[nb][l_k4+0][l_r+32] = ra1.x; As[nb][l_k4+1][l_r+32] = ra1.y;
-            As[nb][l_k4+2][l_r+32] = ra1.z; As[nb][l_k4+3][l_r+32] = ra1.w;
-            Bs[nb][l_k4+0][l_r] = rb0.x; Bs[nb][l_k4+1][l_r] = rb0.y;
-            Bs[nb][l_k4+2][l_r] = rb0.z; Bs[nb][l_k4+3][l_r] = rb0.w;
-            Bs[nb][l_k4+0][l_r+32] = rb1.x; Bs[nb][l_k4+1][l_r+32] = rb1.y;
-            Bs[nb][l_k4+2][l_r+32] = rb1.z; Bs[nb][l_k4+3][l_r+32] = rb1.w;
-        }
-        __syncthreads();
-    }
-    #pragma unroll
-    for (int r = 0; r < 4; ++r) {
-        float4 o = make_float4(acc[r][0], acc[r][1], acc[r][2], acc[r][3]);
-        *(float4*)(C + (size_t)(b0 + tr*4 + r)*256 + j0 + tc*4) = o;
-    }
-}
-
-__global__ __launch_bounds__(256) void ln_relu_kernel(
-        const float* __restrict__ P,
-        const float* __restrict__ bias,
+__global__ __launch_bounds__(256) void ln_relu_fb_kernel(
+        const float* __restrict__ P, const float* __restrict__ bias,
         const float* __restrict__ g, const float* __restrict__ be,
         float* __restrict__ Y) {
     int b = blockIdx.x, tid = threadIdx.x;
@@ -477,9 +783,68 @@
     yr[tid+768] = fmaxf((v3-mu)*inv*g[tid+768] + be[tid+768], 0.f);
 }
 
-__global__ __launch_bounds__(256) void ln_out_kernel(
-        const float* __restrict__ P,
-        const float* __restrict__ bias,
+__global__ __launch_bounds__(256) void gemm2_fb_kernel(
+        const float* __restrict__ Amat, const float* __restrict__ W,
+        float* __restrict__ Cpart) {
+    __shared__ __align__(16) char smem[27000];
+    float (*As)[32][36] = (float(*)[32][36])smem;
+    float (*Bs)[32][68] = (float(*)[32][68])(smem + 9216);
+    const int b0 = blockIdx.x * 32, j0 = blockIdx.y * 64;
+    const int kbase = blockIdx.z * 128;
+    float* C = Cpart + (size_t)blockIdx.z * 512 * 256;
+    const int tid = threadIdx.x;
+    const int tr = tid >> 4, tc = tid & 15;
+    const int l_r = tid >> 3, l_k4 = (tid & 7) * 4;
+    float4 ra0, rb0, rb1;
+    float acc[2][4] = {};
+    {
+        const int k0 = kbase;
+        ra0 = *(const float4*)(Amat + (size_t)(b0 + l_r)*1024 + k0 + l_k4);
+        rb0 = *(const float4*)(W + (size_t)(j0 + l_r)*1024 + k0 + l_k4);
+        rb1 = *(const float4*)(W + (size_t)(j0 + l_r + 32)*1024 + k0 + l_k4);
+        As[0][l_k4+0][l_r] = ra0.x; As[0][l_k4+1][l_r] = ra0.y;
+        As[0][l_k4+2][l_r] = ra0.z; As[0][l_k4+3][l_r] = ra0.w;
+        Bs[0][l_k4+0][l_r] = rb0.x; Bs[0][l_k4+1][l_r] = rb0.y;
+        Bs[0][l_k4+2][l_r] = rb0.z; Bs[0][l_k4+3][l_r] = rb0.w;
+        Bs[0][l_k4+0][l_r+32] = rb1.x; Bs[0][l_k4+1][l_r+32] = rb1.y;
+        Bs[0][l_k4+2][l_r+32] = rb1.z; Bs[0][l_k4+3][l_r+32] = rb1.w;
+    }
+    __syncthreads();
+    for (int s = 0; s < 4; ++s) {
+        if (s < 3) {
+            const int k0 = kbase + (s+1)*32;
+            ra0 = *(const float4*)(Amat + (size_t)(b0 + l_r)*1024 + k0 + l_k4);
+            rb0 = *(const float4*)(W + (size_t)(j0 + l_r)*1024 + k0 + l_k4);
+            rb1 = *(const float4*)(W + (size_t)(j0 + l_r + 32)*1024 + k0 + l_k4);
+        }
+        const int bf = s & 1;
+        #pragma unroll
+        for (int kk = 0; kk < 32; ++kk) {
+            float a0 = As[bf][kk][tr*2], a1 = As[bf][kk][tr*2+1];
+            float4 bv = *(const float4*)&Bs[bf][kk][tc*4];
+            acc[0][0] += a0*bv.x; acc[0][1] += a0*bv.y; acc[0][2] += a0*bv.z; acc[0][3] += a0*bv.w;
+            acc[1][0] += a1*bv.x; acc[1][1] += a1*bv.y; acc[1][2] += a1*bv.z; acc[1][3] += a1*bv.w;
+        }
+        if (s < 3) {
+            const int nb = bf ^ 1;
+            As[nb][l_k4+0][l_r] = ra0.x; As[nb][l_k4+1][l_r] = ra0.y;
+            As[nb][l_k4+2][l_r] = ra0.z; As[nb][l_k4+3][l_r] = ra0.w;
+            Bs[nb][l_k4+0][l_r] = rb0.x; Bs[nb][l_k4+1][l_r] = rb0.y;
+            Bs[nb][l_k4+2][l_r] = rb0.z; Bs[nb][l_k4+3][l_r] = rb0.w;
+            Bs[nb][l_k4+0][l_r+32] = rb1.x; Bs[nb][l_k4+1][l_r+32] = rb1.y;
+            Bs[nb][l_k4+2][l_r+32] = rb1.z; Bs[nb][l_k4+3][l_r+32] = rb1.w;
+        }
+        __syncthreads();
+    }
+    #pragma unroll
+    for (int r = 0; r < 2; ++r) {
+        float4 o = make_float4(acc[r][0], acc[r][1], acc[r][2], acc[r][3]);
+        *(float4*)(C + (size_t)(b0 + tr*2 + r)*256 + j0 + tc*4) = o;
+    }
+}
+
+__global__ __launch_bounds__(256) void ln_out_fb_kernel(
+        const float* __restrict__ P, const float* __restrict__ bias,
         const float* __restrict__ g, const float* __restrict__ be,
         float* __restrict__ Y) {
     int b = blockIdx.x, tid = threadIdx.x;
@@ -535,49 +900,63 @@
     float* out = (float*)d_out;
     float* ws  = (float*)d_ws;
 
-    float2* Uc = (float2*)ws;
-    float2* Cc = Uc + 288;
-    float* A0   = ws + 1024;
-    float* m0   = ws + 7168;
-    float* A1   = ws + 13312;
-    float* m1   = ws + 19456;
-    float* Yraw = ws + 25600;
-    float* h1T  = ws + 32768;
-    float* h1   = ws + 294912;
-    float* h2T  = ws + 32768;
-    float* t3p  = ws + 557056;
-    float* t3n  = ws + 1605632;
-    float* t4p  = ws + 557056;
-
-    hipLaunchKernelGGL(consts_kernel, dim3(1), dim3(256), 0, stream,
-                       rot0, ent0, rot1, ent1, Uc, Cc);
-
-    hipLaunchKernelGGL(encode_rm_kernel, dim3(128), dim3(256), 0, stream,
-                       x, qWe0, qbe0, Yraw);
-    hipLaunchKernelGGL(bn_tanh_kernel, dim3(1), dim3(512), 0, stream,
-                       Yraw, qgi0, qbi0, A0);
-    hipLaunchKernelGGL(qsim_kernel, dim3(512), dim3(256), 0, stream,
-                       A0, Uc, Cc, 0, m0);
-    hipLaunchKernelGGL(decode_kernel, dim3(512), dim3(512), 0, stream,
-                       m0, qWd0, qbd0, qgo0, qbo0, h1T);
-    hipLaunchKernelGGL(transpose512_kernel, dim3(64), dim3(256), 0, stream,
-                       h1T, h1);
-
-    hipLaunchKernelGGL(encode_rm_kernel, dim3(128), dim3(256), 0, stream,
-                       h1, qWe1, qbe1, Yraw);
-    hipLaunchKernelGGL(bn_tanh_kernel, dim3(1), dim3(512), 0, stream,
-                       Yraw, qgi1, qbi1, A1);
-    hipLaunchKernelGGL(qsim_kernel, dim3(512), dim3(256), 0, stream,
-                       A1, Uc, Cc, 1, m1);
-    hipLaunchKernelGGL(decode_kernel, dim3(512), dim3(512), 0, stream,
-                       m1, qWd1, qbd1, qgo1, qbo1, h2T);
-
-    hipLaunchKernelGGL(gemm1_kernel, dim3(8, 16, 2), dim3(256), 0, stream,
-                       h2T, W2, t3p);
-    hipLaunchKernelGGL(ln_relu_kernel, dim3(512), dim3(256), 0, stream,
-                       t3p, b2, ln2g, ln2b, t3n);
-    hipLaunchKernelGGL(gemm2_kernel, dim3(8, 4, 8), dim3(256), 0, stream,
-                       t3n, Wo, t4p);
-    hipLaunchKernelGGL(ln_out_kernel, dim3(512), dim3(256), 0, stream,
-                       t4p, bo, lnog, lnob, out);
-}
+    float2* Uc   = (float2*)ws;
+    float2* Cc   = Uc + 288;
+    float* Yraw0 = ws + 1024;
+    float* m0    = ws + 7680;
+    float* Yraw1 = ws + 14336;
+    float* m1    = ws + 20992;
+    float* A0    = ws + 27648;
+    float* A1    = ws + 33792;
+    float* h1T   = ws + 65536;
+    float* h1    = ws + 327680;
+    float* h2T   = ws + 589824;
+    float* t3p   = ws + 851968;
+    float* t3n   = ws + 2949120;
+    float* t4p   = ws + 3473408;
+
+    MegaParams p;
+    p.x = x;
+    p.qWe0=qWe0; p.qbe0=qbe0; p.qgi0=qgi0; p.qbi0=qbi0; p.rot0=rot0; p.ent0=ent0;
+    p.qWd0=qWd0; p.qbd0=qbd0; p.qgo0=qgo0; p.qbo0=qbo0;
+    p.qWe1=qWe1; p.qbe1=qbe1; p.qgi1=qgi1; p.qbi1=qbi1; p.rot1=rot1; p.ent1=ent1;
+    p.qWd1=qWd1; p.qbd1=qbd1; p.qgo1=qgo1; p.qbo1=qbo1;
+    p.W2=W2; p.b2=b2; p.ln2g=ln2g; p.ln2b=ln2b; p.Wo=Wo; p.bo=bo; p.lnog=lnog; p.lnob=lnob;
+    p.Uc=Uc; p.Cc=Cc; p.Yraw0=Yraw0; p.m0=m0; p.Yraw1=Yraw1; p.m1=m1;
+    p.h1T=h1T; p.h2T=h2T; p.t3p=t3p; p.t3n=t3n; p.t4p=t4p; p.out=out;
+
+    void* kargs[] = { (void*)&p };
+    hipError_t err = hipLaunchCooperativeKernel((const void*)mega_kernel,
+                                                dim3(512), dim3(256), kargs, 0, stream);
+    if (err != hipSuccess) {
+        (void)hipGetLastError();
+        hipLaunchKernelGGL(consts_kernel, dim3(1), dim3(256), 0, stream,
+                           rot0, ent0, rot1, ent1, Uc, Cc);
+        hipLaunchKernelGGL(encode_rm_kernel, dim3(128), dim3(256), 0, stream,
+                           x, qWe0, qbe0, Yraw0);
+        hipLaunchKernelGGL(bn_tanh_kernel, dim3(1), dim3(512), 0, stream,
+                           Yraw0, qgi0, qbi0, A0);
+        hipLaunchKernelGGL(qsim_kernel, dim3(512), dim3(256), 0, stream,
+                           A0, Uc, Cc, 0, m0);
+        hipLaunchKernelGGL(decode_kernel, dim3(512), dim3(512), 0, stream,
+                           m0, qWd0, qbd0, qgo0, qbo0, h1T);
+        hipLaunchKernelGGL(transpose512_kernel, dim3(64), dim3(256), 0, stream,
+                           h1T, h1);
+        hipLaunchKernelGGL(encode_rm_kernel, dim3(128), dim3(256), 0, stream,
+                           h1, qWe1, qbe1, Yraw0);
+        hipLaunchKernelGGL(bn_tanh_kernel, dim3(1), dim3(512), 0, stream,
+                           Yraw0, qgi1, qbi1, A1);
+        hipLaunchKernelGGL(qsim_kernel, dim3(512), dim3(256), 0, stream,
+                           A1, Uc, Cc, 1, m1);
+        hipLaunchKernelGGL(decode_kernel, dim3(512), dim3(512), 0, stream,
+                           m1, qWd1, qbd1, qgo1, qbo1, h2T);
+        hipLaunchKernelGGL(gemm1_fb_kernel, dim3(8, 16, 2), dim3(256), 0, stream,
+                           h2T, W2, t3p);
+        hipLaunchKernelGGL(ln_relu_fb_kernel, dim3(512), dim3(256), 0, stream,
+                           t3p, b2, ln2g, ln2b, t3n);
+        hipLaunchKernelGGL(gemm2_fb_kernel, dim3(16, 4, 8), dim3(256), 0, stream,
+                           t3n, Wo, t4p);
+        hipLaunchKernelGGL(ln_out_fb_kernel, dim3(512), dim3(256), 0, stream,
+                           t4p, bo, lnog, lnob, out);
+    }
+}
```

New measurement: 760.4 us. 223% more time.
